# Optimization experiments

Hardware: AMD Instinct MI355X
Metric: run time of the kernel (lower is better)

The kernel has to match this reference:

```python
import jax, jax.numpy as jnp
import numpy as np

T, B, C = 512, 4, 256   # seq, batch, in_features
R = 256                 # reduce_dim (== in_features == out_features, required by original view/matmul)
OUT = 256
NE = 64                 # n experts / codebook size
D = R * OUT             # 65536, centroid dimension
TAU = 1.0               # gumbel temperature
DECAY = 0.999           # EMA decay
COMMIT = 0.25           # commitment scale


def setup_inputs() -> dict:
    key = jax.random.key(0)
    ks = jax.random.split(key, 6)
    x = jax.random.normal(ks[0], (T, B, C), dtype=jnp.float32)
    # uniform noise for gumbel sampling (kept as input for determinism)
    u_noise = jax.random.uniform(ks[1], (T * B, NE), dtype=jnp.float32,
                                 minval=1e-6, maxval=1.0 - 1e-6)
    W_map = jax.random.normal(ks[2], (D, C), dtype=jnp.float32) * 0.02   # xavier-ish
    b_map = jnp.zeros((D,), jnp.float32)
    pw_w1 = jax.random.normal(ks[3], (1, 1, R, C), dtype=jnp.float32) * (1.0 / np.sqrt(R))
    pw_B = jnp.zeros((1, 1, OUT), jnp.float32)   # 'constant' bias mode, init 0
    centroids = jax.random.normal(ks[4], (NE, D), dtype=jnp.float32) * 0.5  # init_centroids std
    return {"x": x, "u_noise": u_noise, "W_map": W_map, "b_map": b_map,
            "pw_w1": pw_w1, "pw_B": pw_B, "centroids": centroids}


def reference(x, u_noise, W_map, b_map, pw_w1, pw_B, centroids):
    N = T * B
    # key projection: [N, D]
    keyf = x.reshape(N, C) @ W_map.T + b_map
    kd = jax.lax.stop_gradient(keyf)  # assign() uses points.data

    # squared euclidean cdist: ||p||^2 + ||c||^2 - 2 p c^T   [N, NE]
    d2 = (kd * kd).sum(1, keepdims=True) \
         + (centroids * centroids).sum(1)[None, :] \
         - 2.0 * (kd @ centroids.T)

    # gumbel-softmax routing (soft, hard=False); resp detached (depends only on data)
    g = -jnp.log(-jnp.log(u_noise))
    resp = jax.nn.softmax((-d2 + g) / TAU, axis=-1)  # [N, NE]

    # vectorized EMA centroid update (original loops over experts; math identical,
    # mean_assigned[i] = mean_n resp[n,i]*key[n] = (resp^T @ key)/N), detached in original
    mean_assigned = (resp.T @ kd) / N                # [NE, D]
    centroids_new = DECAY * centroids + (1.0 - DECAY) * mean_assigned

    # quantized U-vectors from UPDATED centroids (update precedes matmul in original)
    quantized = resp @ centroids_new                 # [N, D]

    # euclid commitment loss (quantized detached)
    loss = COMMIT * jnp.mean((keyf - jax.lax.stop_gradient(quantized)) ** 2)

    # dynamic per-token weight: w = quantized.view(T,B,R,C) @ pw_w1  -> [T,B,R,C]
    w2 = jnp.einsum('tbik,kj->tbij', quantized.reshape(T, B, R, C), pw_w1[0, 0])
    # apply to input: [T,B,R,C] @ [T,B,C] -> [T,B,OUT]  (R == OUT)
    out = jnp.einsum('tbij,tbj->tbi', w2, x) + pw_B  # constant bias broadcasts
    return (out, loss)
```

## Files before the change

kernel.cpp:

```cpp
#include <hip/hip_runtime.h>
#include <hip/hip_bf16.h>

constexpr int N_TOK = 2048;
constexpr int C_    = 256;
constexpr int NE    = 64;
constexpr int D_    = 65536;
constexpr float DECAYF = 0.999f;
constexpr float OMD    = 0.001f;
constexpr float ALPHA  = OMD / 2048.0f;
constexpr float RTHRESH = 1e-5f;
constexpr int CHMAX = 8448;
constexpr int SA_GRIDX = 512;

using bf16x8 = __attribute__((ext_vector_type(8))) short;
using f32x4  = __attribute__((ext_vector_type(4))) float;
using u16 = unsigned short;

constexpr size_t OFF_S     = 0;
constexpr size_t OFF_XSUM  = 65536;
constexpr size_t OFF_G     = 65792;
constexpr size_t OFF_M     = 131328;
constexpr size_t OFF_WB    = 147712;
constexpr size_t OFF_BB    = 147968;
constexpr size_t OFF_SUMR  = 147984;
constexpr size_t OFF_A     = 148048;
constexpr size_t OFF_CC0   = 164432;
constexpr size_t OFF_RR    = 168528;
constexpr size_t OFF_CNT   = 172624;
constexpr size_t OFF_CN2   = 172688;
constexpr size_t OFF_CB    = 172752;
constexpr size_t OFF_TSLOT = 172816;
constexpr size_t ZFLOATS   = 174864;
constexpr size_t OFF_RESP  = 174864;
constexpr size_t OFF_AG    = 174864;
constexpr size_t OFF_MA    = 191248;
constexpr size_t OFF_AGA   = 195344;
constexpr size_t OFF_AWB   = 199440;
constexpr size_t OFF_CHE   = 199504;
constexpr size_t OFF_CHB   = 207952;
constexpr size_t OFF_NCH   = 216400;
constexpr size_t OFF_Y     = 305936;
constexpr size_t OFF_CNEW  = 830224;
constexpr size_t OFF_TIDX  = 5024528;
constexpr size_t OFF_TOKR  = 5155600;
constexpr size_t OFF_WTH   = 5286672;
constexpr size_t OFF_SCG   = 13675280;
constexpr size_t OFF_SCC   = 16296720;
constexpr size_t WS_FAST2_END = 18393872;

__device__ __forceinline__ unsigned pack_bf2(float a, float b) {
  __hip_bfloat16 ha = __float2bfloat16(a), hb = __float2bfloat16(b);
  unsigned short ua = *reinterpret_cast<unsigned short*>(&ha);
  unsigned short ub = *reinterpret_cast<unsigned short*>(&hb);
  return (unsigned)ua | ((unsigned)ub << 16);
}

__global__ __launch_bounds__(256) void k_pre(const float* __restrict__ bmap,
    const float* __restrict__ x, const float* __restrict__ W,
    float* __restrict__ bb, float* __restrict__ xsum, float* __restrict__ Wb) {
  int bx = blockIdx.x;
  int t = threadIdx.x;
  if (bx < 4) {
    int base = bx * 16384 + t;
    float s = 0.f;
    for (int q = 0; q < 64; q++) { float v = bmap[base + q * 256]; s = fmaf(v, v, s); }
    __shared__ float red[256];
    red[t] = s;
    __syncthreads();
    for (int k = 128; k > 0; k >>= 1) {
      if (t < k) red[t] += red[t + k];
      __syncthreads();
    }
    if (t == 0) atomicAdd(&bb[0], red[0]);
  } else if (bx < 36) {
    int n0 = (bx - 4) * 64;
    float s = 0.f;
    for (int n = 0; n < 64; n++) s += x[(n0 + n) * C_ + t];
    atomicAdd(&xsum[t], s);
  } else {
    int d0 = (bx - 36) * 256;
    __shared__ float bs[256];
    __shared__ int any;
    if (t == 0) any = 0;
    __syncthreads();
    float bv = bmap[d0 + t];
    bs[t] = bv;
    if (bv != 0.f) any = 1;
    __syncthreads();
    if (any == 0) return;
    float s = 0.f;
    for (int d = 0; d < 256; d++) s = fmaf(bs[d], W[(size_t)(d0 + d) * C_ + t], s);
    atomicAdd(&Wb[t], s);
  }
}

template<int KCHUNK>
__device__ __forceinline__ void gemm_tt_tile(
    const float* __restrict__ Aop, int lda, int ca,
    const float* __restrict__ Bop, int ldb, int cb,
    int d0, float* __restrict__ Out, int ldo, int ro, int co) {
  __shared__ float Wa[32][68], Wb[32][68];
  int t = threadIdx.x;
  int tx = t & 15, ty = t >> 4;
  int lr = t >> 3, lc = (t & 7) * 8;
  float acc[4][4] = {};
  for (int dk = 0; dk < KCHUNK; dk += 32) {
    const float* Arow = &Aop[(size_t)(d0 + dk + lr) * lda + ca];
    const float* Brow = &Bop[(size_t)(d0 + dk + lr) * ldb + cb];
    float4 a0 = *(const float4*)&Arow[lc];
    float4 a1 = *(const float4*)&Arow[lc + 4];
    float4 b0 = *(const float4*)&Brow[lc];
    float4 b1 = *(const float4*)&Brow[lc + 4];
    __syncthreads();
    *(float4*)&Wa[lr][lc]     = a0;
    *(float4*)&Wa[lr][lc + 4] = a1;
    *(float4*)&Wb[lr][lc]     = b0;
    *(float4*)&Wb[lr][lc + 4] = b1;
    __syncthreads();
    #pragma unroll
    for (int k = 0; k < 32; k++) {
      float4 ra4 = *(const float4*)&Wa[k][ty * 4];
      float4 rb4 = *(const float4*)&Wb[k][tx * 4];
      float ra[4] = {ra4.x, ra4.y, ra4.z, ra4.w};
      float rb[4] = {rb4.x, rb4.y, rb4.z, rb4.w};
      #pragma unroll
      for (int i = 0; i < 4; i++)
        #pragma unroll
        for (int j = 0; j < 4; j++)
          acc[i][j] = fmaf(ra[i], rb[j], acc[i][j]);
    }
  }
  #pragma unroll
  for (int i = 0; i < 4; i++)
    #pragma unroll
    for (int j = 0; j < 4; j++)
      atomicAdd(&Out[(size_t)(ro + ty * 4 + i) * ldo + co + tx * 4 + j], acc[i][j]);
}

__global__ __launch_bounds__(256) void k_Tw(const float* __restrict__ W,
    u16* __restrict__ wth) {
  __shared__ float Ls[32][257];
  int t = threadIdx.x;
  int d0 = blockIdx.x * 32;
  int r = t >> 3, c8 = (t & 7) * 32;
  #pragma unroll
  for (int q = 0; q < 8; q++) {
    float4 v = *(const float4*)&W[(size_t)(d0 + r) * 256 + c8 + q * 4];
    Ls[r][c8 + q * 4 + 0] = v.x; Ls[r][c8 + q * 4 + 1] = v.y;
    Ls[r][c8 + q * 4 + 2] = v.z; Ls[r][c8 + q * 4 + 3] = v.w;
  }
  __syncthreads();
  int dq = (t & 3) * 8;
  #pragma unroll
  for (int pQ = 0; pQ < 4; pQ++) {
    int c = pQ * 64 + (t >> 2);
    unsigned hw[4];
    #pragma unroll
    for (int q = 0; q < 4; q++)
      hw[q] = pack_bf2(Ls[dq + 2 * q][c], Ls[dq + 2 * q + 1][c]);
    size_t o = (size_t)c * 65536 + d0 + dq;
    *(uint4*)&wth[o] = make_uint4(hw[0], hw[1], hw[2], hw[3]);
  }
}

__global__ __launch_bounds__(256) void k_G3(const u16* __restrict__ wth,
    float* __restrict__ part) {
  int kb = blockIdx.x;
  int p = blockIdx.y;
  int ti = 0, rem0 = p;
  while (rem0 >= 4 - ti) { rem0 -= 4 - ti; ti++; }
  int tj = ti + rem0;
  bool two = (ti != tj);
  const u16* srcA = wth + (size_t)(ti * 64) * 65536;
  const u16* srcB = wth + (size_t)(tj * 64) * 65536;
  __shared__ __align__(16) u16 Ta[8 * 68 * 8], Tb[8 * 68 * 8];
  int t = threadIdx.x, l = t & 63, w = t >> 6;
  int m0 = w * 16, lm = l & 15, g = l >> 4;
  int scol = t >> 3, skseg = t & 7;
  f32x4 acc[4] = {};
  for (int cc = 0; cc < 16; cc++) {
    int k0 = kb * 1024 + cc * 64;
    __syncthreads();
    {
      uint4 a0 = *(const uint4*)(srcA + (size_t)scol * 65536 + k0 + skseg * 8);
      uint4 a1 = *(const uint4*)(srcA + (size_t)(scol + 32) * 65536 + k0 + skseg * 8);
      *(uint4*)(Ta + (skseg * 68 + scol) * 8) = a0;
      *(uint4*)(Ta + (skseg * 68 + scol + 32) * 8) = a1;
      if (two) {
        uint4 b0 = *(const uint4*)(srcB + (size_t)scol * 65536 + k0 + skseg * 8);
        uint4 b1 = *(const uint4*)(srcB + (size_t)(scol + 32) * 65536 + k0 + skseg * 8);
        *(uint4*)(Tb + (skseg * 68 + scol) * 8) = b0;
        *(uint4*)(Tb + (skseg * 68 + scol + 32) * 8) = b1;
      }
    }
    __syncthreads();
    const u16* TBp = two ? Tb : Ta;
    #pragma unroll
    for (int ks = 0; ks < 2; ks++) {
      int kq = ks * 4 + g;
      bf16x8 av = *(const bf16x8*)(Ta + (kq * 68 + m0 + lm) * 8);
      #pragma unroll
      for (int j = 0; j < 4; j++) {
        bf16x8 bv = *(const bf16x8*)(TBp + (kq * 68 + j * 16 + lm) * 8);
        acc[j] = __builtin_amdgcn_mfma_f32_16x16x32_bf16(av, bv, acc[j], 0, 0, 0);
      }
    }
  }
  float* pp = &part[((size_t)p * 64 + kb) * 4096];
  #pragma unroll
  for (int j = 0; j < 4; j++)
    #pragma unroll
    for (int r = 0; r < 4; r++)
      pp[(m0 + (l >> 4) * 4 + r) * 64 + j * 16 + lm] = acc[j][r];
}

__global__ __launch_bounds__(256) void k_Gslow(const float* __restrict__ W,
    float* __restrict__ part) {
  int p = blockIdx.y;
  int ti = 0, rem0 = p;
  while (rem0 >= 4 - ti) { rem0 -= 4 - ti; ti++; }
  int tj = ti + rem0;
  int c1 = ti * 64, c2 = tj * 64;
  int d0 = blockIdx.x * 1024;
  __shared__ unsigned short Wat[64][40], Wbt[64][40];
  int t = threadIdx.x;
  int h = t >> 7;
  int rem = t & 127;
  int k2 = rem >> 3;
  int c4b = rem & 7;
  int cbase = h ? c2 : c1;
  unsigned short (*dst)[40] = h ? Wbt : Wat;
  int l = t & 63, w = t >> 6;
  int m0 = w * 16;
  int lm = l & 15, q8 = (l >> 4) * 8;
  f32x4 acc[4] = {};
  for (int dk = 0; dk < 1024; dk += 32) {
    __syncthreads();
    #pragma unroll
    for (int it = 0; it < 2; it++) {
      int c4 = c4b + it * 8;
      const float* rp = &W[(size_t)(d0 + dk + k2 * 2) * C_ + cbase + c4 * 4];
      float4 g0 = *(const float4*)rp;
      float4 g1 = *(const float4*)(rp + C_);
      *(unsigned*)&dst[c4 * 4 + 0][k2 * 2] = pack_bf2(g0.x, g1.x);
      *(unsigned*)&dst[c4 * 4 + 1][k2 * 2] = pack_bf2(g0.y, g1.y);
      *(unsigned*)&dst[c4 * 4 + 2][k2 * 2] = pack_bf2(g0.z, g1.z);
      *(unsigned*)&dst[c4 * 4 + 3][k2 * 2] = pack_bf2(g0.w, g1.w);
    }
    __syncthreads();
    bf16x8 av = *(const bf16x8*)&Wat[m0 + lm][q8];
    #pragma unroll
    for (int j = 0; j < 4; j++) {
      bf16x8 bv = *(const bf16x8*)&Wbt[j * 16 + lm][q8];
      acc[j] = __builtin_amdgcn_mfma_f32_16x16x32_bf16(av, bv, acc[j], 0, 0, 0);
    }
  }
  float* pp = &part[((size_t)p * 64 + blockIdx.x) * 4096];
  #pragma unroll
  for (int j = 0; j < 4; j++)
    #pragma unroll
    for (int r = 0; r < 4; r++)
      pp[(m0 + (l >> 4) * 4 + r) * 64 + j * 16 + lm] = acc[j][r];
}

__global__ __launch_bounds__(256) void k_Gred(const float* __restrict__ part,
    float* __restrict__ G) {
  int p = blockIdx.y;
  int ti = 0, rem0 = p;
  while (rem0 >= 4 - ti) { rem0 -= 4 - ti; ti++; }
  int tj = ti + rem0;
  int i = blockIdx.x * 256 + threadIdx.x;
  const float* base = part + (size_t)p * 64 * 4096 + i;
  float s = 0.f;
  for (int kb = 0; kb < 64; kb++) s += base[(size_t)kb * 4096];
  int r = i >> 6, c = i & 63;
  G[(ti * 64 + r) * C_ + tj * 64 + c] = s;
  if (ti != tj) G[(tj * 64 + c) * C_ + ti * 64 + r] = s;
}

__global__ __launch_bounds__(256) void k_Mred(const float* __restrict__ mpart,
    float* __restrict__ M) {
  int i = blockIdx.x * 256 + threadIdx.x;
  int kb0 = blockIdx.y * 64;
  float s = 0.f;
  #pragma unroll 8
  for (int kb = 0; kb < 64; kb++) s += mpart[(size_t)(kb0 + kb) * 16384 + i];
  atomicAdd(&M[i], s);
}

__global__ __launch_bounds__(256) void k_CCred(const float* __restrict__ part,
    float* __restrict__ CC0) {
  int i = (blockIdx.x & 15) * 256 + threadIdx.x;
  int kb0 = (blockIdx.x >> 4) * 64;
  float s = 0.f;
  #pragma unroll 8
  for (int kb = 0; kb < 64; kb++) s += part[(size_t)(kb0 + kb) * 4096 + i];
  atomicAdd(&CC0[i], s);
}

__global__ __launch_bounds__(256) void k_redAll(const float* __restrict__ gp,
    const float* __restrict__ mp, const float* __restrict__ cp,
    float* __restrict__ G, float* __restrict__ M, float* __restrict__ CC0) {
  int bx = blockIdx.x;
  if (bx < 160) {
    int p = bx / 16, ib = bx % 16;
    int ti = 0, rem0 = p;
    while (rem0 >= 4 - ti) { rem0 -= 4 - ti; ti++; }
    int tj = ti + rem0;
    int i = ib * 256 + threadIdx.x;
    const float* base = gp + (size_t)p * 64 * 4096 + i;
    float s = 0.f;
    for (int kb = 0; kb < 64; kb++) s += base[(size_t)kb * 4096];
    int r = i >> 6, c = i & 63;
    G[(ti * 64 + r) * C_ + tj * 64 + c] = s;
    if (ti != tj) G[(tj * 64 + c) * C_ + ti * 64 + r] = s;
  } else if (bx < 416) {
    int idx = bx - 160;
    int i = (idx & 63) * 256 + threadIdx.x;
    int kb0 = (idx >> 6) * 64;
    float s = 0.f;
    #pragma unroll 8
    for (int kb = 0; kb < 64; kb++) s += mp[(size_t)(kb0 + kb) * 16384 + i];
    atomicAdd(&M[i], s);
  } else {
    int idx = bx - 416;
    int i = (idx & 15) * 256 + threadIdx.x;
    int kb0 = (idx >> 4) * 64;
    float s = 0.f;
    #pragma unroll 8
    for (int kb = 0; kb < 64; kb++) s += cp[(size_t)(kb0 + kb) * 4096 + i];
    atomicAdd(&CC0[i], s);
  }
}


__global__ __launch_bounds__(256) void k_AR(const float* __restrict__ resp,
    const float* __restrict__ x, float* __restrict__ A, float* __restrict__ RR) {
  if (blockIdx.y < 4)
    gemm_tt_tile<256>(resp, NE, 0, x, C_, blockIdx.y * 64, blockIdx.x * 256,
                      A, C_, 0, blockIdx.y * 64);
  else
    gemm_tt_tile<256>(resp, NE, 0, resp, NE, 0, blockIdx.x * 256, RR, NE, 0, 0);
}

__global__ __launch_bounds__(256) void k_sr(const float* __restrict__ resp,
    float* __restrict__ sumresp) {
  int e = threadIdx.x & 63, part = threadIdx.x >> 6;
  int n0 = blockIdx.x * 256 + part * 64;
  float s = 0.f;
  for (int n = n0; n < n0 + 64; n++) s += resp[n * NE + e];
  __shared__ float red[256];
  red[threadIdx.x] = s;
  __syncthreads();
  if (part == 0)
    atomicAdd(&sumresp[e], red[e] + red[64 + e] + red[128 + e] + red[192 + e]);
}

__global__ __launch_bounds__(256) void k_M(const float* __restrict__ cen,
    const float* __restrict__ W, float* __restrict__ mpart) {
  int kb = blockIdx.x;
  int c0 = blockIdx.y * 64;
  int d0 = kb * 256;
  __shared__ float As[32][68];
  __shared__ float Bs[32][68];
  int t = threadIdx.x;
  int tx = t & 15, ty = t >> 4;
  int e = t >> 2, dg = t & 3;
  int lr = t >> 3, lc = (t & 7) * 8;
  float acc[4][4] = {};
  for (int dk = 0; dk < 256; dk += 32) {
    const float* cr = &cen[(size_t)e * D_ + d0 + dk];
    float4 cv0 = *(const float4*)&cr[dg * 4];
    float4 cv1 = *(const float4*)&cr[16 + dg * 4];
    const float* wr = &W[(size_t)(d0 + dk + lr) * C_ + c0];
    float4 w0 = *(const float4*)&wr[lc];
    float4 w1 = *(const float4*)&wr[lc + 4];
    __syncthreads();
    As[dg * 4 + 0][e] = cv0.x; As[dg * 4 + 1][e] = cv0.y;
    As[dg * 4 + 2][e] = cv0.z; As[dg * 4 + 3][e] = cv0.w;
    As[16 + dg * 4 + 0][e] = cv1.x; As[16 + dg * 4 + 1][e] = cv1.y;
    As[16 + dg * 4 + 2][e] = cv1.z; As[16 + dg * 4 + 3][e] = cv1.w;
    *(float4*)&Bs[lr][lc]     = w0;
    *(float4*)&Bs[lr][lc + 4] = w1;
    __syncthreads();
    #pragma unroll 8
    for (int k = 0; k < 32; k++) {
      float4 ra4 = *(const float4*)&As[k][ty * 4];
      float4 rb4 = *(const float4*)&Bs[k][tx * 4];
      float ra[4] = {ra4.x, ra4.y, ra4.z, ra4.w};
      float rb[4] = {rb4.x, rb4.y, rb4.z, rb4.w};
      #pragma unroll
      for (int i = 0; i < 4; i++)
        #pragma unroll
        for (int j = 0; j < 4; j++)
          acc[i][j] = fmaf(ra[i], rb[j], acc[i][j]);
    }
  }
  float* pp = &mpart[(size_t)kb * 16384];
  #pragma unroll
  for (int i = 0; i < 4; i++)
    *(float4*)&pp[(ty * 4 + i) * C_ + c0 + tx * 4] = *(float4*)&acc[i][0];
}

__global__ __launch_bounds__(256) void k_CCp(const float* __restrict__ cen,
    const float* __restrict__ bmap, float* __restrict__ part,
    float* __restrict__ cb) {
  int d0 = blockIdx.x * 128;
  __shared__ float cs[32][68];
  __shared__ float red[256];
  int t = threadIdx.x;
  int e = t >> 2, dg = t & 3;
  int tx = t & 15, ty = t >> 4;
  float acc[4][4] = {};
  float cbp = 0.f;
  for (int dk = 0; dk < 128; dk += 32) {
    const float* cr = &cen[(size_t)e * D_ + d0 + dk];
    float4 v0 = *(const float4*)&cr[dg * 4];
    float4 v1 = *(const float4*)&cr[16 + dg * 4];
    const float* br = &bmap[d0 + dk];
    float4 b0 = *(const float4*)&br[dg * 4];
    float4 b1 = *(const float4*)&br[16 + dg * 4];
    cbp += v0.x * b0.x + v0.y * b0.y + v0.z * b0.z + v0.w * b0.w
         + v1.x * b1.x + v1.y * b1.y + v1.z * b1.z + v1.w * b1.w;
    __syncthreads();
    cs[dg * 4 + 0][e] = v0.x; cs[dg * 4 + 1][e] = v0.y;
    cs[dg * 4 + 2][e] = v0.z; cs[dg * 4 + 3][e] = v0.w;
    cs[16 + dg * 4 + 0][e] = v1.x; cs[16 + dg * 4 + 1][e] = v1.y;
    cs[16 + dg * 4 + 2][e] = v1.z; cs[16 + dg * 4 + 3][e] = v1.w;
    __syncthreads();
    #pragma unroll
    for (int k = 0; k < 32; k++) {
      float4 ra4 = *(const float4*)&cs[k][ty * 4];
      float4 rb4 = *(const float4*)&cs[k][tx * 4];
      float ra[4] = {ra4.x, ra4.y, ra4.z, ra4.w};
      float rb[4] = {rb4.x, rb4.y, rb4.z, rb4.w};
      #pragma unroll
      for (int i = 0; i < 4; i++)
        #pragma unroll
        for (int j = 0; j < 4; j++)
          acc[i][j] = fmaf(ra[i], rb[j], acc[i][j]);
    }
  }
  float* pp = &part[(size_t)blockIdx.x * 4096];
  #pragma unroll
  for (int i = 0; i < 4; i++)
    *(float4*)&pp[(ty * 4 + i) * 64 + tx * 4] = *(float4*)&acc[i][0];
  red[t] = cbp;
  __syncthreads();
  if (t < 64)
    atomicAdd(&cb[t], red[t * 4] + red[t * 4 + 1] + red[t * 4 + 2] + red[t * 4 + 3]);
}

__global__ __launch_bounds__(256) void k_ygs(const float* __restrict__ x,
    const float* __restrict__ pw, const float* __restrict__ G,
    float* __restrict__ y, float* __restrict__ gsum) {
  int n0 = blockIdx.x * 64;
  bool isg = blockIdx.y >= 4;
  int k0 = (blockIdx.y & 3) * 64;
  const float* B = isg ? G : pw;
  __shared__ float Xs[64][17], Ps[64][17];
  __shared__ float red[256];
  int t = threadIdx.x;
  int tx = t & 15, ty = t >> 4;
  int r = t >> 2, q4 = (t & 3) * 4;
  float acc[4][4] = {};
  for (int j0 = 0; j0 < 256; j0 += 16) {
    float4 va = *(const float4*)&x[(n0 + r) * C_ + j0 + q4];
    float4 vb = *(const float4*)&B[(k0 + r) * C_ + j0 + q4];
    __syncthreads();
    Xs[r][q4] = va.x; Xs[r][q4+1] = va.y; Xs[r][q4+2] = va.z; Xs[r][q4+3] = va.w;
    Ps[r][q4] = vb.x; Ps[r][q4+1] = vb.y; Ps[r][q4+2] = vb.z; Ps[r][q4+3] = vb.w;
    __syncthreads();
    #pragma unroll
    for (int k = 0; k < 16; k++) {
      float ra[4], rb[4];
      #pragma unroll
      for (int i = 0; i < 4; i++) ra[i] = Xs[ty*4 + i][k];
      #pragma unroll
      for (int j = 0; j < 4; j++) rb[j] = Ps[tx*4 + j][k];
      #pragma unroll
      for (int i = 0; i < 4; i++)
        #pragma unroll
        for (int j = 0; j < 4; j++)
          acc[i][j] = fmaf(ra[i], rb[j], acc[i][j]);
    }
  }
  if (!isg) {
    #pragma unroll
    for (int i = 0; i < 4; i++)
      #pragma unroll
      for (int j = 0; j < 4; j++)
        y[(n0 + ty*4 + i) * C_ + k0 + tx*4 + j] = acc[i][j];
  } else {
    float s = 0.f;
    #pragma unroll
    for (int i = 0; i < 4; i++) {
      float4 xv = *(const float4*)&x[(size_t)(n0 + ty*4 + i) * C_ + k0 + tx*4];
      s += acc[i][0]*xv.x + acc[i][1]*xv.y + acc[i][2]*xv.z + acc[i][3]*xv.w;
    }
    red[t] = s;
    __syncthreads();
    for (int k = 128; k > 0; k >>= 1) {
      if (t < k) red[t] += red[t + k];
      __syncthreads();
    }
    if (t == 0) atomicAdd(gsum, red[0]);
  }
}

__global__ __launch_bounds__(256) void k_resp(const float* __restrict__ x,
    const float* __restrict__ u, const float* __restrict__ M,
    const float* __restrict__ CC0, const float* __restrict__ cb,
    float* __restrict__ resp) {
  int t = threadIdx.x;
  int tok = t >> 6, e = t & 63;
  int n = blockIdx.x * 4 + tok;
  __shared__ float xs[4][256];
  *(float4*)&xs[tok][e * 4] = *(const float4*)&x[n * C_ + e * 4];
  __syncthreads();
  const float* Me = M + e * C_;
  const float* xr = xs[tok];
  float s = 0.f;
  #pragma unroll 8
  for (int j = 0; j < 256; j += 4) {
    float4 m4 = *(const float4*)&Me[j];
    s = fmaf(xr[j],   m4.x, s);
    s = fmaf(xr[j+1], m4.y, s);
    s = fmaf(xr[j+2], m4.z, s);
    s = fmaf(xr[j+3], m4.w, s);
  }
  float uu = u[n * NE + e];
  float g = -logf(-logf(uu));
  float logit = 2.0f * (s + cb[e]) - CC0[e * 65] + g;
  float m = logit;
  for (int off = 32; off > 0; off >>= 1) m = fmaxf(m, __shfl_xor(m, off));
  float ex = expf(logit - m);
  float sum = ex;
  for (int off = 32; off > 0; off >>= 1) sum += __shfl_xor(sum, off);
  resp[n * NE + e] = ex / sum;
}

__global__ __launch_bounds__(256) void k_route(const float* __restrict__ resp,
    unsigned int* __restrict__ cnt, int* __restrict__ tokidx,
    float* __restrict__ tokr, int* __restrict__ tslot) {
  int n = blockIdx.x * 256 + threadIdx.x;
  int s = 0;
  #pragma unroll 4
  for (int e = 0; e < NE; e++) {
    float r = resp[n * NE + e];
    if (r > RTHRESH) {
      unsigned pos = atomicAdd(&cnt[e], 1u);
      tokidx[e * 2048 + pos] = n;
      tokr[e * 2048 + pos] = r;
      s++;
    }
  }
  tslot[n] = s;
}

__global__ __launch_bounds__(256) void k_plan(const unsigned int* __restrict__ cnt,
    int* __restrict__ che, int* __restrict__ chb, int* __restrict__ nch) {
  __shared__ int cbase[65];
  __shared__ int ncs[64];
  int t = threadIdx.x;
  if (t < 64) ncs[t] = ((int)cnt[t] + 15) >> 4;
  __syncthreads();
  if (t == 0) {
    int s = 0;
    for (int e = 0; e < 64; e++) { cbase[e] = s; s += ncs[e]; }
    cbase[64] = s;
    nch[0] = s < CHMAX ? s : CHMAX;
  }
  __syncthreads();
  for (int e = 0; e < 64; e++) {
    int b0 = cbase[e], nc = cbase[e + 1] - b0;
    for (int i = t; i < nc; i += 256) {
      int idx = b0 + i;
      if (idx < CHMAX) { che[idx] = e; chb[idx] = i * 16; }
    }
  }
}

__global__ __launch_bounds__(256) void k_ag(const float* __restrict__ A,
    const float* __restrict__ G, const float* __restrict__ Wb,
    float* __restrict__ AG, float* __restrict__ AWb) {
  int e = blockIdx.x, c = threadIdx.x;
  float s = 0.f;
  for (int cp = 0; cp < C_; cp++) s = fmaf(A[e * C_ + cp], G[cp * C_ + c], s);
  AG[e * C_ + c] = s;
  float p = A[e * C_ + c] * Wb[c];
  __shared__ float red[256];
  red[c] = p;
  __syncthreads();
  for (int k = 128; k > 0; k >>= 1) {
    if (c < k) red[c] += red[c + k];
    __syncthreads();
  }
  if (c == 0) AWb[e] = red[0];
}

__global__ __launch_bounds__(256) void k_small64(const float* __restrict__ M,
    const float* __restrict__ A, const float* __restrict__ AG,
    float* __restrict__ MA, float* __restrict__ AGA) {
  int e = blockIdx.x;
  int f = threadIdx.x >> 2, q = threadIdx.x & 3;
  float s1 = 0.f, s2 = 0.f;
  for (int c = q * 64; c < q * 64 + 64; c++) {
    float a = A[f * C_ + c];
    s1 = fmaf(M[e * C_ + c], a, s1);
    s2 = fmaf(AG[e * C_ + c], a, s2);
  }
  __shared__ float r1[256], r2[256];
  r1[threadIdx.x] = s1; r2[threadIdx.x] = s2;
  __syncthreads();
  if (q == 0) {
    MA[e * NE + f]  = r1[f*4] + r1[f*4+1] + r1[f*4+2] + r1[f*4+3];
    AGA[e * NE + f] = r2[f*4] + r2[f*4+1] + r2[f*4+2] + r2[f*4+3];
  }
}

__global__ __launch_bounds__(256) void k_cnew(const float* __restrict__ A,
    const float* __restrict__ sumresp, const float* __restrict__ cen,
    const float* __restrict__ bmap, const float* __restrict__ W,
    float* __restrict__ cnew) {
  int d0 = blockIdx.x * 64;
  __shared__ __align__(16) u16 Abf[64 * 264];
  __shared__ __align__(16) u16 Wt[64 * 264];
  __shared__ float srs[64];
  int t = threadIdx.x, l = t & 63;
  int m0 = (t >> 6) * 16, lm = l & 15, g = l >> 4;
  {
    int e = t >> 2, c0 = (t & 3) * 64;
    const float* ar = &A[e * C_ + c0];
    u16* dst = &Abf[e * 264 + c0];
    #pragma unroll
    for (int q = 0; q < 8; q++) {
      float4 v0 = *(const float4*)&ar[q * 8];
      float4 v1 = *(const float4*)&ar[q * 8 + 4];
      *(uint4*)&dst[q * 8] = make_uint4(pack_bf2(v0.x, v0.y), pack_bf2(v0.z, v0.w),
                                        pack_bf2(v1.x, v1.y), pack_bf2(v1.z, v1.w));
    }
    int r = t >> 2;
    const float* wr = &W[(size_t)(d0 + r) * C_ + c0];
    u16* wdst = &Wt[r * 264 + c0];
    #pragma unroll
    for (int q = 0; q < 8; q++) {
      float4 v0 = *(const float4*)&wr[q * 8];
      float4 v1 = *(const float4*)&wr[q * 8 + 4];
      *(uint4*)&wdst[q * 8] = make_uint4(pack_bf2(v0.x, v0.y), pack_bf2(v0.z, v0.w),
                                         pack_bf2(v1.x, v1.y), pack_bf2(v1.z, v1.w));
    }
    if (t < 64) srs[t] = sumresp[t];
  }
  __syncthreads();
  f32x4 acc[4] = {};
  #pragma unroll
  for (int kk = 0; kk < 8; kk++) {
    bf16x8 av = *(const bf16x8*)&Abf[(m0 + lm) * 264 + kk * 32 + g * 8];
    #pragma unroll
    for (int j = 0; j < 4; j++) {
      bf16x8 bv = *(const bf16x8*)&Wt[(j * 16 + lm) * 264 + kk * 32 + g * 8];
      acc[j] = __builtin_amdgcn_mfma_f32_16x16x32_bf16(av, bv, acc[j], 0, 0, 0);
    }
  }
  #pragma unroll
  for (int j = 0; j < 4; j++) {
    int d = d0 + j * 16 + lm;
    float bv = bmap[d];
    #pragma unroll
    for (int r = 0; r < 4; r++) {
      int e = m0 + g * 4 + r;
      size_t o = (size_t)e * D_ + d;
      cnew[o] = DECAYF * cen[o] + ALPHA * (acc[j][r] + srs[e] * bv);
    }
  }
}

__global__ __launch_bounds__(256) void k_bias(const float* __restrict__ pwB, float* __restrict__ out) {
  int idx = blockIdx.x * 256 + threadIdx.x;
  out[idx] = pwB[idx & 255];
}

__global__ __launch_bounds__(256) void k_sA(const int* __restrict__ che,
    const int* __restrict__ chb, const int* __restrict__ nch,
    const unsigned int* __restrict__ cnt, const int* __restrict__ tokidx,
    const float* __restrict__ tokr, const int* __restrict__ tslot,
    const float* __restrict__ y, const float* __restrict__ cnew,
    float* __restrict__ out) {
  int nchv = nch[0];
  int i0 = blockIdx.y * 128;
  __shared__ int nsh[16]; __shared__ float rsh[16]; __shared__ int wsh[16];
  __shared__ float Ys[16][260];
  __shared__ float Bs[32][132];
  int t = threadIdx.x;
  for (int ch = blockIdx.x; ch < nchv; ch += SA_GRIDX) {
    int e = che[ch], base = chb[ch];
    int c = (int)cnt[e];
    __syncthreads();
    if (t < 16) {
      int idx = base + t;
      if (idx < c) {
        int n = tokidx[e * 2048 + idx];
        nsh[t] = n; rsh[t] = tokr[e * 2048 + idx]; wsh[t] = tslot[n];
      } else { nsh[t] = 0; rsh[t] = 0.f; wsh[t] = 2; }
    }
    __syncthreads();
    {
      int row = t >> 4, c0 = (t & 15) * 16;
      const float* yr = &y[nsh[row] * C_ + c0];
      float4 v0 = *(const float4*)&yr[0];
      float4 v1 = *(const float4*)&yr[4];
      float4 v2 = *(const float4*)&yr[8];
      float4 v3 = *(const float4*)&yr[12];
      *(float4*)&Ys[row][c0]      = v0;
      *(float4*)&Ys[row][c0 + 4]  = v1;
      *(float4*)&Ys[row][c0 + 8]  = v2;
      *(float4*)&Ys[row][c0 + 12] = v3;
    }
    int tx = t & 31, ty = t >> 5;
    int br = t >> 1, bk = (t & 1) * 16;
    float acc[2][4] = {};
    for (int k0 = 0; k0 < 256; k0 += 32) {
      const float* Brow = &cnew[(size_t)e * D_ + (size_t)(i0 + br) * C_ + k0 + bk];
      float4 b0 = *(const float4*)&Brow[0];
      float4 b1 = *(const float4*)&Brow[4];
      float4 b2 = *(const float4*)&Brow[8];
      float4 b3 = *(const float4*)&Brow[12];
      __syncthreads();
      Bs[bk+0][br]  = b0.x; Bs[bk+1][br]  = b0.y; Bs[bk+2][br]  = b0.z; Bs[bk+3][br]  = b0.w;
      Bs[bk+4][br]  = b1.x; Bs[bk+5][br]  = b1.y; Bs[bk+6][br]  = b1.z; Bs[bk+7][br]  = b1.w;
      Bs[bk+8][br]  = b2.x; Bs[bk+9][br]  = b2.y; Bs[bk+10][br] = b2.z; Bs[bk+11][br] = b2.w;
      Bs[bk+12][br] = b3.x; Bs[bk+13][br] = b3.y; Bs[bk+14][br] = b3.z; Bs[bk+15][br] = b3.w;
      __syncthreads();
      #pragma unroll
      for (int kk = 0; kk < 32; kk++) {
        float a0 = Ys[ty*2 + 0][k0 + kk];
        float a1 = Ys[ty*2 + 1][k0 + kk];
        float4 bv = *(const float4*)&Bs[kk][tx*4];
        acc[0][0] = fmaf(a0, bv.x, acc[0][0]); acc[0][1] = fmaf(a0, bv.y, acc[0][1]);
        acc[0][2] = fmaf(a0, bv.z, acc[0][2]); acc[0][3] = fmaf(a0, bv.w, acc[0][3]);
        acc[1][0] = fmaf(a1, bv.x, acc[1][0]); acc[1][1] = fmaf(a1, bv.y, acc[1][1]);
        acc[1][2] = fmaf(a1, bv.z, acc[1][2]); acc[1][3] = fmaf(a1, bv.w, acc[1][3]);
      }
    }
    #pragma unroll
    for (int i = 0; i < 2; i++) {
      int tk = ty*2 + i;
      float r = rsh[tk];
      if (r == 0.f) continue;
      int n = nsh[tk];
      float* op = &out[n * C_ + i0 + tx*4];
      if (wsh[tk] == 1) {
        float4 cur = *(const float4*)op;
        cur.x += r * acc[i][0]; cur.y += r * acc[i][1];
        cur.z += r * acc[i][2]; cur.w += r * acc[i][3];
        *(float4*)op = cur;
      } else {
        atomicAdd(op + 0, r * acc[i][0]);
        atomicAdd(op + 1, r * acc[i][1]);
        atomicAdd(op + 2, r * acc[i][2]);
        atomicAdd(op + 3, r * acc[i][3]);
      }
    }
  }
}

__global__ __launch_bounds__(256) void k_finalize(
    const float* __restrict__ gsum, const float* __restrict__ M,
    const float* __restrict__ A, const float* __restrict__ AG,
    const float* __restrict__ CC0, const float* __restrict__ RR,
    const float* __restrict__ MA, const float* __restrict__ AGA,
    const float* __restrict__ Xsum, const float* __restrict__ Wb,
    const float* __restrict__ bb, const float* __restrict__ sr,
    const float* __restrict__ cb, const float* __restrict__ AWb,
    float* __restrict__ out) {
  int t = threadIdx.x;
  float a_gs = (t == 0) ? gsum[0] : 0.f;
  float a_am = 0.f, a_aag = 0.f;
  for (int i = t; i < 16384; i += 256) {
    float a = A[i];
    a_am  = fmaf(M[i], a, a_am);
    a_aag = fmaf(AG[i], a, a_aag);
  }
  float a_cc = 0.f, a_ma = 0.f, a_aga = 0.f, a_cbsr = 0.f, a_awbsr = 0.f, a_srsr = 0.f;
  for (int p = t; p < 4096; p += 256) {
    float r = RR[p];
    int e = p >> 6, f = p & 63;
    float srf = sr[f];
    a_cc    = fmaf(r, CC0[p], a_cc);
    a_ma    = fmaf(r, MA[p], a_ma);
    a_aga   = fmaf(r, AGA[p], a_aga);
    a_cbsr  = fmaf(r * cb[e], srf, a_cbsr);
    a_awbsr = fmaf(r * AWb[e], srf, a_awbsr);
    a_srsr  = fmaf(r * sr[e], srf, a_srsr);
  }
  float a_xw = Xsum[t] * Wb[t];
  float a_srcb = 0.f, a_srawb = 0.f, a_sr2 = 0.f;
  if (t < 64) { float s = sr[t]; a_srcb = s * cb[t]; a_srawb = s * AWb[t]; a_sr2 = s * s; }
  float v[13] = {a_gs, a_am, a_aag, a_cc, a_ma, a_aga, a_cbsr, a_awbsr, a_srsr,
                 a_xw, a_srcb, a_srawb, a_sr2};
  __shared__ float red[256];
  __shared__ float tot[13];
  for (int q = 0; q < 13; q++) {
    red[t] = v[q];
    __syncthreads();
    for (int s2 = 128; s2 > 0; s2 >>= 1) {
      if (t < s2) red[t] += red[t + s2];
      __syncthreads();
    }
    if (t == 0) tot[q] = red[0];
    __syncthreads();
  }
  if (t == 0) {
    const float q = DECAYF, al = ALPHA;
    float bbv = bb[0];
    float sumkeyf2 = tot[0] + 2.f * tot[9] + 2048.f * bbv;
    float cross = q * (tot[1] + tot[10]) + al * (tot[2] + 2.f * tot[11] + bbv * tot[12]);
    float sumq2 = q*q * tot[3] + 2.f*q*al * (tot[4] + tot[6])
                + al*al * (tot[5] + 2.f * tot[7] + bbv * tot[8]);
    out[524288] = (0.25f / (2048.0f * 65536.0f)) * (sumkeyf2 - 2.f * cross + sumq2);
  }
}

extern "C" void kernel_launch(void* const* d_in, const int* in_sizes, int n_in,
                              void* d_out, int out_size, void* d_ws, size_t ws_size,
                              hipStream_t stream) {
  const float* x    = (const float*)d_in[0];
  const float* u    = (const float*)d_in[1];
  const float* Wm   = (const float*)d_in[2];
  const float* bmap = (const float*)d_in[3];
  const float* pw   = (const float*)d_in[4];
  const float* pwB  = (const float*)d_in[5];
  const float* cen  = (const float*)d_in[6];
  float* out = (float*)d_out;
  float* ws  = (float*)d_ws;

  float* Xsum    = ws + OFF_XSUM;
  float* G       = ws + OFF_G;
  float* M       = ws + OFF_M;
  float* Wb      = ws + OFF_WB;
  float* bb      = ws + OFF_BB;
  float* gsum    = ws + OFF_BB + 1;
  float* sumresp = ws + OFF_SUMR;
  float* A       = ws + OFF_A;
  float* CC0     = ws + OFF_CC0;
  float* RR      = ws + OFF_RR;
  unsigned int* cnt = (unsigned int*)(ws + OFF_CNT);
  float* cb      = ws + OFF_CB;
  int*   tslot   = (int*)(ws + OFF_TSLOT);
  float* resp    = ws + OFF_RESP;
  float* AG      = ws + OFF_AG;
  float* MA      = ws + OFF_MA;
  float* AGA     = ws + OFF_AGA;
  float* AWb     = ws + OFF_AWB;
  int*   che     = (int*)(ws + OFF_CHE);
  int*   chb     = (int*)(ws + OFF_CHB);
  int*   nch     = (int*)(ws + OFF_NCH);
  float* y       = ws + OFF_Y;
  float* cnew    = ws + OFF_CNEW;
  float* scratch = ws + OFF_CNEW;
  int*   tokidx  = (int*)(ws + OFF_TIDX);
  float* tokr    = ws + OFF_TOKR;
  u16*   wth     = (u16*)(ws + OFF_WTH);
  float* sc_g    = ws + OFF_SCG;
  float* sc_cc   = ws + OFF_SCC;

  bool fast2 = ws_size >= (size_t)WS_FAST2_END * sizeof(float);

  hipMemsetAsync(d_ws, 0, ZFLOATS * sizeof(float), stream);

  k_pre<<<292, 256, 0, stream>>>(bmap, x, Wm, bb, Xsum, Wb);
  if (fast2) {
    k_Tw<<<2048, 256, 0, stream>>>(Wm, wth);
    k_G3<<<dim3(64, 10), 256, 0, stream>>>(wth, sc_g);
    k_M<<<dim3(256, 4), 256, 0, stream>>>(cen, Wm, scratch);
    k_CCp<<<512, 256, 0, stream>>>(cen, bmap, sc_cc, cb);
    k_redAll<<<544, 256, 0, stream>>>(sc_g, scratch, sc_cc, G, M, CC0);
  } else {
    k_Gslow<<<dim3(64, 10), 256, 0, stream>>>(Wm, scratch);
    k_Gred<<<dim3(16, 10), 256, 0, stream>>>(scratch, G);
    k_M<<<dim3(256, 4), 256, 0, stream>>>(cen, Wm, scratch);
    k_Mred<<<dim3(64, 4), 256, 0, stream>>>(scratch, M);
    k_CCp<<<512, 256, 0, stream>>>(cen, bmap, scratch, cb);
    k_CCred<<<128, 256, 0, stream>>>(scratch, CC0);
  }
  k_ygs<<<dim3(32, 8), 256, 0, stream>>>(x, pw, G, y, gsum);
  k_resp<<<512, 256, 0, stream>>>(x, u, M, CC0, cb, resp);
  k_route<<<8, 256, 0, stream>>>(resp, cnt, tokidx, tokr, tslot);
  k_AR<<<dim3(8, 5), 256, 0, stream>>>(resp, x, A, RR);
  k_sr<<<8, 256, 0, stream>>>(resp, sumresp);
  k_plan<<<1, 256, 0, stream>>>(cnt, che, chb, nch);
  k_ag<<<64, 256, 0, stream>>>(A, G, Wb, AG, AWb);
  k_small64<<<64, 256, 0, stream>>>(M, A, AG, MA, AGA);
  k_cnew<<<1024, 256, 0, stream>>>(A, sumresp, cen, bmap, Wm, cnew);
  k_bias<<<2048, 256, 0, stream>>>(pwB, out);
  k_sA<<<dim3(SA_GRIDX, 2), 256, 0, stream>>>(che, chb, nch, cnt, tokidx, tokr,
                                              tslot, y, cnew, out);
  k_finalize<<<1, 256, 0, stream>>>(gsum, M, A, AG, CC0, RR, MA, AGA, Xsum, Wb,
                                    bb, sumresp, cb, AWb, out);
}
```

Baseline: 402.3 us.

## Merge independent stage kernels into block-partitioned fused launches

Collapses roughly a dozen small kernel launches into five multi-role kernels, where the block index decides which sub-task (G Gram tiles, M partials, centroid Gram, y/resp, routing, cnew, scatter) a block runs. The aim is to cut launch overhead and the idle tails between small dependent stages by letting independent work share one grid. In exchange, blocks with very different costs share a launch, shared memory is sized for the largest role, and the slow fallback path looks inconsistent (it launches k_big1 reading wth, which that path never fills).

```diff
diff --git a/kernel.cpp b/kernel.cpp
--- a/kernel.cpp
+++ b/kernel.cpp
@@ -10,13 +10,11 @@
 constexpr float ALPHA  = OMD / 2048.0f;
 constexpr float RTHRESH = 1e-5f;
 constexpr int CHMAX = 8448;
-constexpr int SA_GRIDX = 512;
 
 using bf16x8 = __attribute__((ext_vector_type(8))) short;
 using f32x4  = __attribute__((ext_vector_type(4))) float;
 using u16 = unsigned short;
 
-constexpr size_t OFF_S     = 0;
 constexpr size_t OFF_XSUM  = 65536;
 constexpr size_t OFF_G     = 65792;
 constexpr size_t OFF_M     = 131328;
@@ -27,7 +25,6 @@
 constexpr size_t OFF_CC0   = 164432;
 constexpr size_t OFF_RR    = 168528;
 constexpr size_t OFF_CNT   = 172624;
-constexpr size_t OFF_CN2   = 172688;
 constexpr size_t OFF_CB    = 172752;
 constexpr size_t OFF_TSLOT = 172816;
 constexpr size_t ZFLOATS   = 174864;
@@ -55,16 +52,18 @@
   return (unsigned)ua | ((unsigned)ub << 16);
 }
 
-__global__ __launch_bounds__(256) void k_pre(const float* __restrict__ bmap,
+__global__ __launch_bounds__(256) void k_preTw(const float* __restrict__ bmap,
     const float* __restrict__ x, const float* __restrict__ W,
-    float* __restrict__ bb, float* __restrict__ xsum, float* __restrict__ Wb) {
+    float* __restrict__ bb, float* __restrict__ xsum, float* __restrict__ Wb,
+    u16* __restrict__ wth) {
+  __shared__ __align__(16) char smem[32896];
   int bx = blockIdx.x;
   int t = threadIdx.x;
   if (bx < 4) {
+    float* red = (float*)smem;
     int base = bx * 16384 + t;
     float s = 0.f;
     for (int q = 0; q < 64; q++) { float v = bmap[base + q * 256]; s = fmaf(v, v, s); }
-    __shared__ float red[256];
     red[t] = s;
     __syncthreads();
     for (int k = 128; k > 0; k >>= 1) {
@@ -77,10 +76,10 @@
     float s = 0.f;
     for (int n = 0; n < 64; n++) s += x[(n0 + n) * C_ + t];
     atomicAdd(&xsum[t], s);
-  } else {
+  } else if (bx < 292) {
+    float* bs = (float*)smem;
+    __shared__ int any;
     int d0 = (bx - 36) * 256;
-    __shared__ float bs[256];
-    __shared__ int any;
     if (t == 0) any = 0;
     __syncthreads();
     float bv = bmap[d0 + t];
@@ -91,211 +90,173 @@
     float s = 0.f;
     for (int d = 0; d < 256; d++) s = fmaf(bs[d], W[(size_t)(d0 + d) * C_ + t], s);
     atomicAdd(&Wb[t], s);
-  }
-}
-
-template<int KCHUNK>
-__device__ __forceinline__ void gemm_tt_tile(
-    const float* __restrict__ Aop, int lda, int ca,
-    const float* __restrict__ Bop, int ldb, int cb,
-    int d0, float* __restrict__ Out, int ldo, int ro, int co) {
-  __shared__ float Wa[32][68], Wb[32][68];
+  } else {
+    float (*Ls)[257] = (float(*)[257])smem;
+    int d0 = (bx - 292) * 32;
+    int r = t >> 3, c8 = (t & 7) * 32;
+    #pragma unroll
+    for (int q = 0; q < 8; q++) {
+      float4 v = *(const float4*)&W[(size_t)(d0 + r) * 256 + c8 + q * 4];
+      Ls[r][c8 + q * 4 + 0] = v.x; Ls[r][c8 + q * 4 + 1] = v.y;
+      Ls[r][c8 + q * 4 + 2] = v.z; Ls[r][c8 + q * 4 + 3] = v.w;
+    }
+    __syncthreads();
+    int dq = (t & 3) * 8;
+    #pragma unroll
+    for (int pQ = 0; pQ < 4; pQ++) {
+      int c = pQ * 64 + (t >> 2);
+      unsigned hw[4];
+      #pragma unroll
+      for (int q = 0; q < 4; q++)
+        hw[q] = pack_bf2(Ls[dq + 2 * q][c], Ls[dq + 2 * q + 1][c]);
+      size_t o = (size_t)c * 65536 + d0 + dq;
+      *(uint4*)&wth[o] = make_uint4(hw[0], hw[1], hw[2], hw[3]);
+    }
+  }
+}
+
+__global__ __launch_bounds__(256) void k_big1(const u16* __restrict__ wth,
+    const float* __restrict__ cen, const float* __restrict__ W,
+    const float* __restrict__ bmap, float* __restrict__ gpart,
+    float* __restrict__ mpart, float* __restrict__ cpart, float* __restrict__ cb) {
+  __shared__ __align__(16) char smem[17408];
+  int bx = blockIdx.x;
   int t = threadIdx.x;
-  int tx = t & 15, ty = t >> 4;
-  int lr = t >> 3, lc = (t & 7) * 8;
-  float acc[4][4] = {};
-  for (int dk = 0; dk < KCHUNK; dk += 32) {
-    const float* Arow = &Aop[(size_t)(d0 + dk + lr) * lda + ca];
-    const float* Brow = &Bop[(size_t)(d0 + dk + lr) * ldb + cb];
-    float4 a0 = *(const float4*)&Arow[lc];
-    float4 a1 = *(const float4*)&Arow[lc + 4];
-    float4 b0 = *(const float4*)&Brow[lc];
-    float4 b1 = *(const float4*)&Brow[lc + 4];
-    __syncthreads();
-    *(float4*)&Wa[lr][lc]     = a0;
-    *(float4*)&Wa[lr][lc + 4] = a1;
-    *(float4*)&Wb[lr][lc]     = b0;
-    *(float4*)&Wb[lr][lc + 4] = b1;
-    __syncthreads();
-    #pragma unroll
-    for (int k = 0; k < 32; k++) {
-      float4 ra4 = *(const float4*)&Wa[k][ty * 4];
-      float4 rb4 = *(const float4*)&Wb[k][tx * 4];
-      float ra[4] = {ra4.x, ra4.y, ra4.z, ra4.w};
-      float rb[4] = {rb4.x, rb4.y, rb4.z, rb4.w};
-      #pragma unroll
-      for (int i = 0; i < 4; i++)
+  if (bx < 640) {
+    u16* Ta = (u16*)smem;
+    u16* Tb = Ta + 4352;
+    int kb = bx & 63, p = bx >> 6;
+    int ti = 0, rem0 = p;
+    while (rem0 >= 4 - ti) { rem0 -= 4 - ti; ti++; }
+    int tj = ti + rem0;
+    bool two = (ti != tj);
+    const u16* srcA = wth + (size_t)(ti * 64) * 65536;
+    const u16* srcB = wth + (size_t)(tj * 64) * 65536;
+    int l = t & 63, w = t >> 6;
+    int m0 = w * 16, lm = l & 15, g = l >> 4;
+    int scol = t >> 3, skseg = t & 7;
+    f32x4 acc[4] = {};
+    for (int cc = 0; cc < 16; cc++) {
+      int k0 = kb * 1024 + cc * 64;
+      __syncthreads();
+      {
+        uint4 a0 = *(const uint4*)(srcA + (size_t)scol * 65536 + k0 + skseg * 8);
+        uint4 a1 = *(const uint4*)(srcA + (size_t)(scol + 32) * 65536 + k0 + skseg * 8);
+        *(uint4*)(Ta + (skseg * 68 + scol) * 8) = a0;
+        *(uint4*)(Ta + (skseg * 68 + scol + 32) * 8) = a1;
+        if (two) {
+          uint4 b0 = *(const uint4*)(srcB + (size_t)scol * 65536 + k0 + skseg * 8);
+          uint4 b1 = *(const uint4*)(srcB + (size_t)(scol + 32) * 65536 + k0 + skseg * 8);
+          *(uint4*)(Tb + (skseg * 68 + scol) * 8) = b0;
+          *(uint4*)(Tb + (skseg * 68 + scol + 32) * 8) = b1;
+        }
+      }
+      __syncthreads();
+      const u16* TBp = two ? Tb : Ta;
+      #pragma unroll
+      for (int ks = 0; ks < 2; ks++) {
+        int kq = ks * 4 + g;
+        bf16x8 av = *(const bf16x8*)(Ta + (kq * 68 + m0 + lm) * 8);
         #pragma unroll
-        for (int j = 0; j < 4; j++)
-          acc[i][j] = fmaf(ra[i], rb[j], acc[i][j]);
-    }
-  }
-  #pragma unroll
-  for (int i = 0; i < 4; i++)
+        for (int j = 0; j < 4; j++) {
+          bf16x8 bv = *(const bf16x8*)(TBp + (kq * 68 + j * 16 + lm) * 8);
+          acc[j] = __builtin_amdgcn_mfma_f32_16x16x32_bf16(av, bv, acc[j], 0, 0, 0);
+        }
+      }
+    }
+    float* pp = &gpart[((size_t)p * 64 + kb) * 4096];
     #pragma unroll
     for (int j = 0; j < 4; j++)
-      atomicAdd(&Out[(size_t)(ro + ty * 4 + i) * ldo + co + tx * 4 + j], acc[i][j]);
-}
-
-__global__ __launch_bounds__(256) void k_Tw(const float* __restrict__ W,
-    u16* __restrict__ wth) {
-  __shared__ float Ls[32][257];
-  int t = threadIdx.x;
-  int d0 = blockIdx.x * 32;
-  int r = t >> 3, c8 = (t & 7) * 32;
-  #pragma unroll
-  for (int q = 0; q < 8; q++) {
-    float4 v = *(const float4*)&W[(size_t)(d0 + r) * 256 + c8 + q * 4];
-    Ls[r][c8 + q * 4 + 0] = v.x; Ls[r][c8 + q * 4 + 1] = v.y;
-    Ls[r][c8 + q * 4 + 2] = v.z; Ls[r][c8 + q * 4 + 3] = v.w;
-  }
-  __syncthreads();
-  int dq = (t & 3) * 8;
-  #pragma unroll
-  for (int pQ = 0; pQ < 4; pQ++) {
-    int c = pQ * 64 + (t >> 2);
-    unsigned hw[4];
-    #pragma unroll
-    for (int q = 0; q < 4; q++)
-      hw[q] = pack_bf2(Ls[dq + 2 * q][c], Ls[dq + 2 * q + 1][c]);
-    size_t o = (size_t)c * 65536 + d0 + dq;
-    *(uint4*)&wth[o] = make_uint4(hw[0], hw[1], hw[2], hw[3]);
-  }
-}
-
-__global__ __launch_bounds__(256) void k_G3(const u16* __restrict__ wth,
-    float* __restrict__ part) {
-  int kb = blockIdx.x;
-  int p = blockIdx.y;
-  int ti = 0, rem0 = p;
-  while (rem0 >= 4 - ti) { rem0 -= 4 - ti; ti++; }
-  int tj = ti + rem0;
-  bool two = (ti != tj);
-  const u16* srcA = wth + (size_t)(ti * 64) * 65536;
-  const u16* srcB = wth + (size_t)(tj * 64) * 65536;
-  __shared__ __align__(16) u16 Ta[8 * 68 * 8], Tb[8 * 68 * 8];
-  int t = threadIdx.x, l = t & 63, w = t >> 6;
-  int m0 = w * 16, lm = l & 15, g = l >> 4;
-  int scol = t >> 3, skseg = t & 7;
-  f32x4 acc[4] = {};
-  for (int cc = 0; cc < 16; cc++) {
-    int k0 = kb * 1024 + cc * 64;
-    __syncthreads();
-    {
-      uint4 a0 = *(const uint4*)(srcA + (size_t)scol * 65536 + k0 + skseg * 8);
-      uint4 a1 = *(const uint4*)(srcA + (size_t)(scol + 32) * 65536 + k0 + skseg * 8);
-      *(uint4*)(Ta + (skseg * 68 + scol) * 8) = a0;
-      *(uint4*)(Ta + (skseg * 68 + scol + 32) * 8) = a1;
-      if (two) {
-        uint4 b0 = *(const uint4*)(srcB + (size_t)scol * 65536 + k0 + skseg * 8);
-        uint4 b1 = *(const uint4*)(srcB + (size_t)(scol + 32) * 65536 + k0 + skseg * 8);
-        *(uint4*)(Tb + (skseg * 68 + scol) * 8) = b0;
-        *(uint4*)(Tb + (skseg * 68 + scol + 32) * 8) = b1;
-      }
-    }
-    __syncthreads();
-    const u16* TBp = two ? Tb : Ta;
-    #pragma unroll
-    for (int ks = 0; ks < 2; ks++) {
-      int kq = ks * 4 + g;
-      bf16x8 av = *(const bf16x8*)(Ta + (kq * 68 + m0 + lm) * 8);
-      #pragma unroll
-      for (int j = 0; j < 4; j++) {
-        bf16x8 bv = *(const bf16x8*)(TBp + (kq * 68 + j * 16 + lm) * 8);
-        acc[j] = __builtin_amdgcn_mfma_f32_16x16x32_bf16(av, bv, acc[j], 0, 0, 0);
-      }
-    }
-  }
-  float* pp = &part[((size_t)p * 64 + kb) * 4096];
-  #pragma unroll
-  for (int j = 0; j < 4; j++)
-    #pragma unroll
-    for (int r = 0; r < 4; r++)
-      pp[(m0 + (l >> 4) * 4 + r) * 64 + j * 16 + lm] = acc[j][r];
-}
-
-__global__ __launch_bounds__(256) void k_Gslow(const float* __restrict__ W,
-    float* __restrict__ part) {
-  int p = blockIdx.y;
-  int ti = 0, rem0 = p;
-  while (rem0 >= 4 - ti) { rem0 -= 4 - ti; ti++; }
-  int tj = ti + rem0;
-  int c1 = ti * 64, c2 = tj * 64;
-  int d0 = blockIdx.x * 1024;
-  __shared__ unsigned short Wat[64][40], Wbt[64][40];
-  int t = threadIdx.x;
-  int h = t >> 7;
-  int rem = t & 127;
-  int k2 = rem >> 3;
-  int c4b = rem & 7;
-  int cbase = h ? c2 : c1;
-  unsigned short (*dst)[40] = h ? Wbt : Wat;
-  int l = t & 63, w = t >> 6;
-  int m0 = w * 16;
-  int lm = l & 15, q8 = (l >> 4) * 8;
-  f32x4 acc[4] = {};
-  for (int dk = 0; dk < 1024; dk += 32) {
-    __syncthreads();
-    #pragma unroll
-    for (int it = 0; it < 2; it++) {
-      int c4 = c4b + it * 8;
-      const float* rp = &W[(size_t)(d0 + dk + k2 * 2) * C_ + cbase + c4 * 4];
-      float4 g0 = *(const float4*)rp;
-      float4 g1 = *(const float4*)(rp + C_);
-      *(unsigned*)&dst[c4 * 4 + 0][k2 * 2] = pack_bf2(g0.x, g1.x);
-      *(unsigned*)&dst[c4 * 4 + 1][k2 * 2] = pack_bf2(g0.y, g1.y);
-      *(unsigned*)&dst[c4 * 4 + 2][k2 * 2] = pack_bf2(g0.z, g1.z);
-      *(unsigned*)&dst[c4 * 4 + 3][k2 * 2] = pack_bf2(g0.w, g1.w);
-    }
-    __syncthreads();
-    bf16x8 av = *(const bf16x8*)&Wat[m0 + lm][q8];
-    #pragma unroll
-    for (int j = 0; j < 4; j++) {
-      bf16x8 bv = *(const bf16x8*)&Wbt[j * 16 + lm][q8];
-      acc[j] = __builtin_amdgcn_mfma_f32_16x16x32_bf16(av, bv, acc[j], 0, 0, 0);
-    }
-  }
-  float* pp = &part[((size_t)p * 64 + blockIdx.x) * 4096];
-  #pragma unroll
-  for (int j = 0; j < 4; j++)
-    #pragma unroll
-    for (int r = 0; r < 4; r++)
-      pp[(m0 + (l >> 4) * 4 + r) * 64 + j * 16 + lm] = acc[j][r];
-}
-
-__global__ __launch_bounds__(256) void k_Gred(const float* __restrict__ part,
-    float* __restrict__ G) {
-  int p = blockIdx.y;
-  int ti = 0, rem0 = p;
-  while (rem0 >= 4 - ti) { rem0 -= 4 - ti; ti++; }
-  int tj = ti + rem0;
-  int i = blockIdx.x * 256 + threadIdx.x;
-  const float* base = part + (size_t)p * 64 * 4096 + i;
-  float s = 0.f;
-  for (int kb = 0; kb < 64; kb++) s += base[(size_t)kb * 4096];
-  int r = i >> 6, c = i & 63;
-  G[(ti * 64 + r) * C_ + tj * 64 + c] = s;
-  if (ti != tj) G[(tj * 64 + c) * C_ + ti * 64 + r] = s;
-}
-
-__global__ __launch_bounds__(256) void k_Mred(const float* __restrict__ mpart,
-    float* __restrict__ M) {
-  int i = blockIdx.x * 256 + threadIdx.x;
-  int kb0 = blockIdx.y * 64;
-  float s = 0.f;
-  #pragma unroll 8
-  for (int kb = 0; kb < 64; kb++) s += mpart[(size_t)(kb0 + kb) * 16384 + i];
-  atomicAdd(&M[i], s);
-}
-
-__global__ __launch_bounds__(256) void k_CCred(const float* __restrict__ part,
-    float* __restrict__ CC0) {
-  int i = (blockIdx.x & 15) * 256 + threadIdx.x;
-  int kb0 = (blockIdx.x >> 4) * 64;
-  float s = 0.f;
-  #pragma unroll 8
-  for (int kb = 0; kb < 64; kb++) s += part[(size_t)(kb0 + kb) * 4096 + i];
-  atomicAdd(&CC0[i], s);
+      #pragma unroll
+      for (int r = 0; r < 4; r++)
+        pp[(m0 + (l >> 4) * 4 + r) * 64 + j * 16 + lm] = acc[j][r];
+  } else if (bx < 1664) {
+    float (*As)[68] = (float(*)[68])smem;
+    float (*Bs)[68] = (float(*)[68])(smem + 8704);
+    int idx = bx - 640;
+    int kb = idx & 255, c0 = (idx >> 8) * 64;
+    int d0 = kb * 256;
+    int tx = t & 15, ty = t >> 4;
+    int e = t >> 2, dg = t & 3;
+    int lr = t >> 3, lc = (t & 7) * 8;
+    float acc[4][4] = {};
+    for (int dk = 0; dk < 256; dk += 32) {
+      const float* cr = &cen[(size_t)e * D_ + d0 + dk];
+      float4 cv0 = *(const float4*)&cr[dg * 4];
+      float4 cv1 = *(const float4*)&cr[16 + dg * 4];
+      const float* wr = &W[(size_t)(d0 + dk + lr) * C_ + c0];
+      float4 w0 = *(const float4*)&wr[lc];
+      float4 w1 = *(const float4*)&wr[lc + 4];
+      __syncthreads();
+      As[dg * 4 + 0][e] = cv0.x; As[dg * 4 + 1][e] = cv0.y;
+      As[dg * 4 + 2][e] = cv0.z; As[dg * 4 + 3][e] = cv0.w;
+      As[16 + dg * 4 + 0][e] = cv1.x; As[16 + dg * 4 + 1][e] = cv1.y;
+      As[16 + dg * 4 + 2][e] = cv1.z; As[16 + dg * 4 + 3][e] = cv1.w;
+      *(float4*)&Bs[lr][lc]     = w0;
+      *(float4*)&Bs[lr][lc + 4] = w1;
+      __syncthreads();
+      #pragma unroll 8
+      for (int k = 0; k < 32; k++) {
+        float4 ra4 = *(const float4*)&As[k][ty * 4];
+        float4 rb4 = *(const float4*)&Bs[k][tx * 4];
+        float ra[4] = {ra4.x, ra4.y, ra4.z, ra4.w};
+        float rb[4] = {rb4.x, rb4.y, rb4.z, rb4.w};
+        #pragma unroll
+        for (int i = 0; i < 4; i++)
+          #pragma unroll
+          for (int j = 0; j < 4; j++)
+            acc[i][j] = fmaf(ra[i], rb[j], acc[i][j]);
+      }
+    }
+    float* pp = &mpart[(size_t)kb * 16384];
+    #pragma unroll
+    for (int i = 0; i < 4; i++)
+      *(float4*)&pp[(ty * 4 + i) * C_ + c0 + tx * 4] = *(float4*)&acc[i][0];
+  } else {
+    float (*cs)[68] = (float(*)[68])smem;
+    float* red = (float*)(smem + 8704);
+    int d0 = (bx - 1664) * 128;
+    int e = t >> 2, dg = t & 3;
+    int tx = t & 15, ty = t >> 4;
+    float acc[4][4] = {};
+    float cbp = 0.f;
+    for (int dk = 0; dk < 128; dk += 32) {
+      const float* cr = &cen[(size_t)e * D_ + d0 + dk];
+      float4 v0 = *(const float4*)&cr[dg * 4];
+      float4 v1 = *(const float4*)&cr[16 + dg * 4];
+      const float* br = &bmap[d0 + dk];
+      float4 b0 = *(const float4*)&br[dg * 4];
+      float4 b1 = *(const float4*)&br[16 + dg * 4];
+      cbp += v0.x * b0.x + v0.y * b0.y + v0.z * b0.z + v0.w * b0.w
+           + v1.x * b1.x + v1.y * b1.y + v1.z * b1.z + v1.w * b1.w;
+      __syncthreads();
+      cs[dg * 4 + 0][e] = v0.x; cs[dg * 4 + 1][e] = v0.y;
+      cs[dg * 4 + 2][e] = v0.z; cs[dg * 4 + 3][e] = v0.w;
+      cs[16 + dg * 4 + 0][e] = v1.x; cs[16 + dg * 4 + 1][e] = v1.y;
+      cs[16 + dg * 4 + 2][e] = v1.z; cs[16 + dg * 4 + 3][e] = v1.w;
+      __syncthreads();
+      #pragma unroll
+      for (int k = 0; k < 32; k++) {
+        float4 ra4 = *(const float4*)&cs[k][ty * 4];
+        float4 rb4 = *(const float4*)&cs[k][tx * 4];
+        float ra[4] = {ra4.x, ra4.y, ra4.z, ra4.w};
+        float rb[4] = {rb4.x, rb4.y, rb4.z, rb4.w};
+        #pragma unroll
+        for (int i = 0; i < 4; i++)
+          #pragma unroll
+          for (int j = 0; j < 4; j++)
+            acc[i][j] = fmaf(ra[i], rb[j], acc[i][j]);
+      }
+    }
+    float* pp = &cpart[(size_t)(bx - 1664) * 4096];
+    #pragma unroll
+    for (int i = 0; i < 4; i++)
+      *(float4*)&pp[(ty * 4 + i) * 64 + tx * 4] = *(float4*)&acc[i][0];
+    red[t] = cbp;
+    __syncthreads();
+    if (t < 64)
+      atomicAdd(&cb[t], red[t * 4] + red[t * 4 + 1] + red[t * 4 + 2] + red[t * 4 + 3]);
+  }
 }
 
 __global__ __launch_bounds__(256) void k_redAll(const float* __restrict__ gp,
@@ -333,434 +294,373 @@
   }
 }
 
-
-__global__ __launch_bounds__(256) void k_AR(const float* __restrict__ resp,
-    const float* __restrict__ x, float* __restrict__ A, float* __restrict__ RR) {
-  if (blockIdx.y < 4)
-    gemm_tt_tile<256>(resp, NE, 0, x, C_, blockIdx.y * 64, blockIdx.x * 256,
-                      A, C_, 0, blockIdx.y * 64);
-  else
-    gemm_tt_tile<256>(resp, NE, 0, resp, NE, 0, blockIdx.x * 256, RR, NE, 0, 0);
-}
-
-__global__ __launch_bounds__(256) void k_sr(const float* __restrict__ resp,
+__global__ __launch_bounds__(256) void k_big2(const float* __restrict__ x,
+    const float* __restrict__ pw, const float* __restrict__ G,
+    const float* __restrict__ u, const float* __restrict__ M,
+    const float* __restrict__ CC0, const float* __restrict__ cb,
+    float* __restrict__ y, float* __restrict__ gsum, float* __restrict__ resp,
+    unsigned int* __restrict__ cnt, int* __restrict__ tokidx,
+    float* __restrict__ tokr, int* __restrict__ tslot,
     float* __restrict__ sumresp) {
-  int e = threadIdx.x & 63, part = threadIdx.x >> 6;
-  int n0 = blockIdx.x * 256 + part * 64;
-  float s = 0.f;
-  for (int n = n0; n < n0 + 64; n++) s += resp[n * NE + e];
-  __shared__ float red[256];
-  red[threadIdx.x] = s;
-  __syncthreads();
-  if (part == 0)
-    atomicAdd(&sumresp[e], red[e] + red[64 + e] + red[128 + e] + red[192 + e]);
-}
-
-__global__ __launch_bounds__(256) void k_M(const float* __restrict__ cen,
-    const float* __restrict__ W, float* __restrict__ mpart) {
-  int kb = blockIdx.x;
-  int c0 = blockIdx.y * 64;
-  int d0 = kb * 256;
-  __shared__ float As[32][68];
-  __shared__ float Bs[32][68];
+  __shared__ __align__(16) char smem[9728];
+  int bx = blockIdx.x;
   int t = threadIdx.x;
-  int tx = t & 15, ty = t >> 4;
-  int e = t >> 2, dg = t & 3;
-  int lr = t >> 3, lc = (t & 7) * 8;
-  float acc[4][4] = {};
-  for (int dk = 0; dk < 256; dk += 32) {
-    const float* cr = &cen[(size_t)e * D_ + d0 + dk];
-    float4 cv0 = *(const float4*)&cr[dg * 4];
-    float4 cv1 = *(const float4*)&cr[16 + dg * 4];
-    const float* wr = &W[(size_t)(d0 + dk + lr) * C_ + c0];
-    float4 w0 = *(const float4*)&wr[lc];
-    float4 w1 = *(const float4*)&wr[lc + 4];
-    __syncthreads();
-    As[dg * 4 + 0][e] = cv0.x; As[dg * 4 + 1][e] = cv0.y;
-    As[dg * 4 + 2][e] = cv0.z; As[dg * 4 + 3][e] = cv0.w;
-    As[16 + dg * 4 + 0][e] = cv1.x; As[16 + dg * 4 + 1][e] = cv1.y;
-    As[16 + dg * 4 + 2][e] = cv1.z; As[16 + dg * 4 + 3][e] = cv1.w;
-    *(float4*)&Bs[lr][lc]     = w0;
-    *(float4*)&Bs[lr][lc + 4] = w1;
-    __syncthreads();
-    #pragma unroll 8
-    for (int k = 0; k < 32; k++) {
-      float4 ra4 = *(const float4*)&As[k][ty * 4];
-      float4 rb4 = *(const float4*)&Bs[k][tx * 4];
-      float ra[4] = {ra4.x, ra4.y, ra4.z, ra4.w};
-      float rb[4] = {rb4.x, rb4.y, rb4.z, rb4.w};
+  if (bx < 256) {
+    float (*Xs)[17] = (float(*)[17])smem;
+    float (*Ps)[17] = (float(*)[17])(smem + 4352);
+    float* red = (float*)(smem + 8704);
+    int n0 = (bx & 31) * 64;
+    int by = bx >> 5;
+    bool isg = by >= 4;
+    int k0 = (by & 3) * 64;
+    const float* B = isg ? G : pw;
+    int tx = t & 15, ty = t >> 4;
+    int r = t >> 2, q4 = (t & 3) * 4;
+    float acc[4][4] = {};
+    for (int j0 = 0; j0 < 256; j0 += 16) {
+      float4 va = *(const float4*)&x[(n0 + r) * C_ + j0 + q4];
+      float4 vb = *(const float4*)&B[(k0 + r) * C_ + j0 + q4];
+      __syncthreads();
+      Xs[r][q4] = va.x; Xs[r][q4+1] = va.y; Xs[r][q4+2] = va.z; Xs[r][q4+3] = va.w;
+      Ps[r][q4] = vb.x; Ps[r][q4+1] = vb.y; Ps[r][q4+2] = vb.z; Ps[r][q4+3] = vb.w;
+      __syncthreads();
+      #pragma unroll
+      for (int k = 0; k < 16; k++) {
+        float ra[4], rb[4];
+        #pragma unroll
+        for (int i = 0; i < 4; i++) ra[i] = Xs[ty*4 + i][k];
+        #pragma unroll
+        for (int j = 0; j < 4; j++) rb[j] = Ps[tx*4 + j][k];
+        #pragma unroll
+        for (int i = 0; i < 4; i++)
+          #pragma unroll
+          for (int j = 0; j < 4; j++)
+            acc[i][j] = fmaf(ra[i], rb[j], acc[i][j]);
+      }
+    }
+    if (!isg) {
       #pragma unroll
       for (int i = 0; i < 4; i++)
         #pragma unroll
         for (int j = 0; j < 4; j++)
-          acc[i][j] = fmaf(ra[i], rb[j], acc[i][j]);
-    }
-  }
-  float* pp = &mpart[(size_t)kb * 16384];
-  #pragma unroll
-  for (int i = 0; i < 4; i++)
-    *(float4*)&pp[(ty * 4 + i) * C_ + c0 + tx * 4] = *(float4*)&acc[i][0];
-}
-
-__global__ __launch_bounds__(256) void k_CCp(const float* __restrict__ cen,
-    const float* __restrict__ bmap, float* __restrict__ part,
-    float* __restrict__ cb) {
-  int d0 = blockIdx.x * 128;
-  __shared__ float cs[32][68];
-  __shared__ float red[256];
-  int t = threadIdx.x;
-  int e = t >> 2, dg = t & 3;
-  int tx = t & 15, ty = t >> 4;
-  float acc[4][4] = {};
-  float cbp = 0.f;
-  for (int dk = 0; dk < 128; dk += 32) {
-    const float* cr = &cen[(size_t)e * D_ + d0 + dk];
-    float4 v0 = *(const float4*)&cr[dg * 4];
-    float4 v1 = *(const float4*)&cr[16 + dg * 4];
-    const float* br = &bmap[d0 + dk];
-    float4 b0 = *(const float4*)&br[dg * 4];
-    float4 b1 = *(const float4*)&br[16 + dg * 4];
-    cbp += v0.x * b0.x + v0.y * b0.y + v0.z * b0.z + v0.w * b0.w
-         + v1.x * b1.x + v1.y * b1.y + v1.z * b1.z + v1.w * b1.w;
-    __syncthreads();
-    cs[dg * 4 + 0][e] = v0.x; cs[dg * 4 + 1][e] = v0.y;
-    cs[dg * 4 + 2][e] = v0.z; cs[dg * 4 + 3][e] = v0.w;
-    cs[16 + dg * 4 + 0][e] = v1.x; cs[16 + dg * 4 + 1][e] = v1.y;
-    cs[16 + dg * 4 + 2][e] = v1.z; cs[16 + dg * 4 + 3][e] = v1.w;
-    __syncthreads();
-    #pragma unroll
-    for (int k = 0; k < 32; k++) {
-      float4 ra4 = *(const float4*)&cs[k][ty * 4];
-      float4 rb4 = *(const float4*)&cs[k][tx * 4];
-      float ra[4] = {ra4.x, ra4.y, ra4.z, ra4.w};
-      float rb[4] = {rb4.x, rb4.y, rb4.z, rb4.w};
-      #pragma unroll
-      for (int i = 0; i < 4; i++)
-        #pragma unroll
-        for (int j = 0; j < 4; j++)
-          acc[i][j] = fmaf(ra[i], rb[j], acc[i][j]);
-    }
-  }
-  float* pp = &part[(size_t)blockIdx.x * 4096];
-  #pragma unroll
-  for (int i = 0; i < 4; i++)
-    *(float4*)&pp[(ty * 4 + i) * 64 + tx * 4] = *(float4*)&acc[i][0];
-  red[t] = cbp;
-  __syncthreads();
-  if (t < 64)
-    atomicAdd(&cb[t], red[t * 4] + red[t * 4 + 1] + red[t * 4 + 2] + red[t * 4 + 3]);
-}
-
-__global__ __launch_bounds__(256) void k_ygs(const float* __restrict__ x,
-    const float* __restrict__ pw, const float* __restrict__ G,
-    float* __restrict__ y, float* __restrict__ gsum) {
-  int n0 = blockIdx.x * 64;
-  bool isg = blockIdx.y >= 4;
-  int k0 = (blockIdx.y & 3) * 64;
-  const float* B = isg ? G : pw;
-  __shared__ float Xs[64][17], Ps[64][17];
-  __shared__ float red[256];
-  int t = threadIdx.x;
-  int tx = t & 15, ty = t >> 4;
-  int r = t >> 2, q4 = (t & 3) * 4;
-  float acc[4][4] = {};
-  for (int j0 = 0; j0 < 256; j0 += 16) {
-    float4 va = *(const float4*)&x[(n0 + r) * C_ + j0 + q4];
-    float4 vb = *(const float4*)&B[(k0 + r) * C_ + j0 + q4];
-    __syncthreads();
-    Xs[r][q4] = va.x; Xs[r][q4+1] = va.y; Xs[r][q4+2] = va.z; Xs[r][q4+3] = va.w;
-    Ps[r][q4] = vb.x; Ps[r][q4+1] = vb.y; Ps[r][q4+2] = vb.z; Ps[r][q4+3] = vb.w;
-    __syncthreads();
-    #pragma unroll
-    for (int k = 0; k < 16; k++) {
-      float ra[4], rb[4];
-      #pragma unroll
-      for (int i = 0; i < 4; i++) ra[i] = Xs[ty*4 + i][k];
-      #pragma unroll
-      for (int j = 0; j < 4; j++) rb[j] = Ps[tx*4 + j][k];
-      #pragma unroll
-      for (int i = 0; i < 4; i++)
-        #pragma unroll
-        for (int j = 0; j < 4; j++)
-          acc[i][j] = fmaf(ra[i], rb[j], acc[i][j]);
-    }
-  }
-  if (!isg) {
-    #pragma unroll
-    for (int i = 0; i < 4; i++)
-      #pragma unroll
-      for (int j = 0; j < 4; j++)
-        y[(n0 + ty*4 + i) * C_ + k0 + tx*4 + j] = acc[i][j];
+          y[(n0 + ty*4 + i) * C_ + k0 + tx*4 + j] = acc[i][j];
+    } else {
+      float s = 0.f;
+      #pragma unroll
+      for (int i = 0; i < 4; i++) {
+        float4 xv = *(const float4*)&x[(size_t)(n0 + ty*4 + i) * C_ + k0 + tx*4];
+        s += acc[i][0]*xv.x + acc[i][1]*xv.y + acc[i][2]*xv.z + acc[i][3]*xv.w;
+      }
+      red[t] = s;
+      __syncthreads();
+      for (int k = 128; k > 0; k >>= 1) {
+        if (t < k) red[t] += red[t + k];
+        __syncthreads();
+      }
+      if (t == 0) atomicAdd(gsum, red[0]);
+    }
   } else {
+    float* xs   = (float*)smem;
+    float* ssum = xs + 1024;
+    int tok = t >> 6, e = t & 63;
+    int n = (bx - 256) * 4 + tok;
+    if (t < 64) ssum[t] = 0.f;
+    *(float4*)&xs[tok * 256 + e * 4] = *(const float4*)&x[n * C_ + e * 4];
+    __syncthreads();
+    const float* Me = M + e * C_;
+    const float* xr = &xs[tok * 256];
     float s = 0.f;
-    #pragma unroll
-    for (int i = 0; i < 4; i++) {
-      float4 xv = *(const float4*)&x[(size_t)(n0 + ty*4 + i) * C_ + k0 + tx*4];
-      s += acc[i][0]*xv.x + acc[i][1]*xv.y + acc[i][2]*xv.z + acc[i][3]*xv.w;
-    }
-    red[t] = s;
-    __syncthreads();
-    for (int k = 128; k > 0; k >>= 1) {
-      if (t < k) red[t] += red[t + k];
-      __syncthreads();
-    }
-    if (t == 0) atomicAdd(gsum, red[0]);
-  }
-}
-
-__global__ __launch_bounds__(256) void k_resp(const float* __restrict__ x,
-    const float* __restrict__ u, const float* __restrict__ M,
-    const float* __restrict__ CC0, const float* __restrict__ cb,
-    float* __restrict__ resp) {
-  int t = threadIdx.x;
-  int tok = t >> 6, e = t & 63;
-  int n = blockIdx.x * 4 + tok;
-  __shared__ float xs[4][256];
-  *(float4*)&xs[tok][e * 4] = *(const float4*)&x[n * C_ + e * 4];
-  __syncthreads();
-  const float* Me = M + e * C_;
-  const float* xr = xs[tok];
-  float s = 0.f;
-  #pragma unroll 8
-  for (int j = 0; j < 256; j += 4) {
-    float4 m4 = *(const float4*)&Me[j];
-    s = fmaf(xr[j],   m4.x, s);
-    s = fmaf(xr[j+1], m4.y, s);
-    s = fmaf(xr[j+2], m4.z, s);
-    s = fmaf(xr[j+3], m4.w, s);
-  }
-  float uu = u[n * NE + e];
-  float g = -logf(-logf(uu));
-  float logit = 2.0f * (s + cb[e]) - CC0[e * 65] + g;
-  float m = logit;
-  for (int off = 32; off > 0; off >>= 1) m = fmaxf(m, __shfl_xor(m, off));
-  float ex = expf(logit - m);
-  float sum = ex;
-  for (int off = 32; off > 0; off >>= 1) sum += __shfl_xor(sum, off);
-  resp[n * NE + e] = ex / sum;
-}
-
-__global__ __launch_bounds__(256) void k_route(const float* __restrict__ resp,
-    unsigned int* __restrict__ cnt, int* __restrict__ tokidx,
-    float* __restrict__ tokr, int* __restrict__ tslot) {
-  int n = blockIdx.x * 256 + threadIdx.x;
-  int s = 0;
-  #pragma unroll 4
-  for (int e = 0; e < NE; e++) {
-    float r = resp[n * NE + e];
-    if (r > RTHRESH) {
+    #pragma unroll 8
+    for (int j = 0; j < 256; j += 4) {
+      float4 m4 = *(const float4*)&Me[j];
+      s = fmaf(xr[j],   m4.x, s);
+      s = fmaf(xr[j+1], m4.y, s);
+      s = fmaf(xr[j+2], m4.z, s);
+      s = fmaf(xr[j+3], m4.w, s);
+    }
+    float uu = u[n * NE + e];
+    float g = -logf(-logf(uu));
+    float logit = 2.0f * (s + cb[e]) - CC0[e * 65] + g;
+    float m = logit;
+    for (int off = 32; off > 0; off >>= 1) m = fmaxf(m, __shfl_xor(m, off));
+    float ex = expf(logit - m);
+    float sum = ex;
+    for (int off = 32; off > 0; off >>= 1) sum += __shfl_xor(sum, off);
+    float r = ex / sum;
+    resp[n * NE + e] = r;
+    bool take = r > RTHRESH;
+    unsigned long long mask = __ballot(take);
+    if (take) {
       unsigned pos = atomicAdd(&cnt[e], 1u);
       tokidx[e * 2048 + pos] = n;
       tokr[e * 2048 + pos] = r;
-      s++;
-    }
-  }
-  tslot[n] = s;
-}
-
-__global__ __launch_bounds__(256) void k_plan(const unsigned int* __restrict__ cnt,
-    int* __restrict__ che, int* __restrict__ chb, int* __restrict__ nch) {
-  __shared__ int cbase[65];
-  __shared__ int ncs[64];
+    }
+    if (e == 0) tslot[n] = (int)__popcll(mask);
+    atomicAdd(&ssum[e], r);
+    __syncthreads();
+    if (t < 64) atomicAdd(&sumresp[t], ssum[t]);
+  }
+}
+
+__global__ __launch_bounds__(256) void k_big3(const float* __restrict__ resp,
+    const float* __restrict__ x, float* __restrict__ A, float* __restrict__ RR,
+    const unsigned int* __restrict__ cnt, int* __restrict__ che,
+    int* __restrict__ chb, int* __restrict__ nch) {
+  __shared__ __align__(16) char smem[17408];
+  int bx = blockIdx.x;
   int t = threadIdx.x;
-  if (t < 64) ncs[t] = ((int)cnt[t] + 15) >> 4;
-  __syncthreads();
-  if (t == 0) {
-    int s = 0;
-    for (int e = 0; e < 64; e++) { cbase[e] = s; s += ncs[e]; }
-    cbase[64] = s;
-    nch[0] = s < CHMAX ? s : CHMAX;
-  }
-  __syncthreads();
-  for (int e = 0; e < 64; e++) {
-    int b0 = cbase[e], nc = cbase[e + 1] - b0;
-    for (int i = t; i < nc; i += 256) {
-      int idx = b0 + i;
-      if (idx < CHMAX) { che[idx] = e; chb[idx] = i * 16; }
-    }
-  }
-}
-
-__global__ __launch_bounds__(256) void k_ag(const float* __restrict__ A,
+  if (bx < 40) {
+    int by = bx >> 3, bxx = bx & 7;
+    const float* Aop = resp; int lda = NE, ca = 0;
+    const float* Bop; int ldb, cbn; float* Out; int ldo, co;
+    if (by < 4) { Bop = x; ldb = C_; cbn = by * 64; Out = A; ldo = C_; co = by * 64; }
+    else        { Bop = resp; ldb = NE; cbn = 0; Out = RR; ldo = NE; co = 0; }
+    int d0 = bxx * 256;
+    float (*Wa)[68] = (float(*)[68])smem;
+    float (*Wb)[68] = (float(*)[68])(smem + 8704);
+    int tx = t & 15, ty = t >> 4;
+    int lr = t >> 3, lc = (t & 7) * 8;
+    float acc[4][4] = {};
+    for (int dk = 0; dk < 256; dk += 32) {
+      const float* Arow = &Aop[(size_t)(d0 + dk + lr) * lda + ca];
+      const float* Brow = &Bop[(size_t)(d0 + dk + lr) * ldb + cbn];
+      float4 a0 = *(const float4*)&Arow[lc];
+      float4 a1 = *(const float4*)&Arow[lc + 4];
+      float4 b0 = *(const float4*)&Brow[lc];
+      float4 b1 = *(const float4*)&Brow[lc + 4];
+      __syncthreads();
+      *(float4*)&Wa[lr][lc]     = a0;
+      *(float4*)&Wa[lr][lc + 4] = a1;
+      *(float4*)&Wb[lr][lc]     = b0;
+      *(float4*)&Wb[lr][lc + 4] = b1;
+      __syncthreads();
+      #pragma unroll
+      for (int k = 0; k < 32; k++) {
+        float4 ra4 = *(const float4*)&Wa[k][ty * 4];
+        float4 rb4 = *(const float4*)&Wb[k][tx * 4];
+        float ra[4] = {ra4.x, ra4.y, ra4.z, ra4.w};
+        float rb[4] = {rb4.x, rb4.y, rb4.z, rb4.w};
+        #pragma unroll
+        for (int i = 0; i < 4; i++)
+          #pragma unroll
+          for (int j = 0; j < 4; j++)
+            acc[i][j] = fmaf(ra[i], rb[j], acc[i][j]);
+      }
+    }
+    #pragma unroll
+    for (int i = 0; i < 4; i++)
+      #pragma unroll
+      for (int j = 0; j < 4; j++)
+        atomicAdd(&Out[(size_t)(ty * 4 + i) * ldo + co + tx * 4 + j], acc[i][j]);
+  } else {
+    int* cbase = (int*)smem;
+    int* ncs   = cbase + 65;
+    if (t < 64) ncs[t] = ((int)cnt[t] + 15) >> 4;
+    __syncthreads();
+    if (t == 0) {
+      int s = 0;
+      for (int e = 0; e < 64; e++) { cbase[e] = s; s += ncs[e]; }
+      cbase[64] = s;
+      nch[0] = s < CHMAX ? s : CHMAX;
+    }
+    __syncthreads();
+    for (int e = 0; e < 64; e++) {
+      int b0 = cbase[e], nc = cbase[e + 1] - b0;
+      for (int i = t; i < nc; i += 256) {
+        int idx = b0 + i;
+        if (idx < CHMAX) { che[idx] = e; chb[idx] = i * 16; }
+      }
+    }
+  }
+}
+
+__global__ __launch_bounds__(256) void k_big4(const float* __restrict__ A,
     const float* __restrict__ G, const float* __restrict__ Wb,
-    float* __restrict__ AG, float* __restrict__ AWb) {
-  int e = blockIdx.x, c = threadIdx.x;
-  float s = 0.f;
-  for (int cp = 0; cp < C_; cp++) s = fmaf(A[e * C_ + cp], G[cp * C_ + c], s);
-  AG[e * C_ + c] = s;
-  float p = A[e * C_ + c] * Wb[c];
-  __shared__ float red[256];
-  red[c] = p;
-  __syncthreads();
-  for (int k = 128; k > 0; k >>= 1) {
-    if (c < k) red[c] += red[c + k];
-    __syncthreads();
-  }
-  if (c == 0) AWb[e] = red[0];
-}
-
-__global__ __launch_bounds__(256) void k_small64(const float* __restrict__ M,
-    const float* __restrict__ A, const float* __restrict__ AG,
-    float* __restrict__ MA, float* __restrict__ AGA) {
-  int e = blockIdx.x;
-  int f = threadIdx.x >> 2, q = threadIdx.x & 3;
-  float s1 = 0.f, s2 = 0.f;
-  for (int c = q * 64; c < q * 64 + 64; c++) {
-    float a = A[f * C_ + c];
-    s1 = fmaf(M[e * C_ + c], a, s1);
-    s2 = fmaf(AG[e * C_ + c], a, s2);
-  }
-  __shared__ float r1[256], r2[256];
-  r1[threadIdx.x] = s1; r2[threadIdx.x] = s2;
-  __syncthreads();
-  if (q == 0) {
-    MA[e * NE + f]  = r1[f*4] + r1[f*4+1] + r1[f*4+2] + r1[f*4+3];
-    AGA[e * NE + f] = r2[f*4] + r2[f*4+1] + r2[f*4+2] + r2[f*4+3];
-  }
-}
-
-__global__ __launch_bounds__(256) void k_cnew(const float* __restrict__ A,
     const float* __restrict__ sumresp, const float* __restrict__ cen,
     const float* __restrict__ bmap, const float* __restrict__ W,
-    float* __restrict__ cnew) {
-  int d0 = blockIdx.x * 64;
-  __shared__ __align__(16) u16 Abf[64 * 264];
-  __shared__ __align__(16) u16 Wt[64 * 264];
-  __shared__ float srs[64];
-  int t = threadIdx.x, l = t & 63;
-  int m0 = (t >> 6) * 16, lm = l & 15, g = l >> 4;
-  {
-    int e = t >> 2, c0 = (t & 3) * 64;
-    const float* ar = &A[e * C_ + c0];
-    u16* dst = &Abf[e * 264 + c0];
-    #pragma unroll
-    for (int q = 0; q < 8; q++) {
-      float4 v0 = *(const float4*)&ar[q * 8];
-      float4 v1 = *(const float4*)&ar[q * 8 + 4];
-      *(uint4*)&dst[q * 8] = make_uint4(pack_bf2(v0.x, v0.y), pack_bf2(v0.z, v0.w),
-                                        pack_bf2(v1.x, v1.y), pack_bf2(v1.z, v1.w));
-    }
-    int r = t >> 2;
-    const float* wr = &W[(size_t)(d0 + r) * C_ + c0];
-    u16* wdst = &Wt[r * 264 + c0];
-    #pragma unroll
-    for (int q = 0; q < 8; q++) {
-      float4 v0 = *(const float4*)&wr[q * 8];
-      float4 v1 = *(const float4*)&wr[q * 8 + 4];
-      *(uint4*)&wdst[q * 8] = make_uint4(pack_bf2(v0.x, v0.y), pack_bf2(v0.z, v0.w),
-                                         pack_bf2(v1.x, v1.y), pack_bf2(v1.z, v1.w));
-    }
-    if (t < 64) srs[t] = sumresp[t];
-  }
-  __syncthreads();
-  f32x4 acc[4] = {};
-  #pragma unroll
-  for (int kk = 0; kk < 8; kk++) {
-    bf16x8 av = *(const bf16x8*)&Abf[(m0 + lm) * 264 + kk * 32 + g * 8];
+    const float* __restrict__ pwB, float* __restrict__ AG,
+    float* __restrict__ AWb, float* __restrict__ cnew, float* __restrict__ out) {
+  __shared__ __align__(16) char smem[67840];
+  int bx = blockIdx.x;
+  int t = threadIdx.x;
+  if (bx < 64) {
+    float* red = (float*)smem;
+    int e = bx, c = t;
+    float s = 0.f;
+    for (int cp = 0; cp < C_; cp++) s = fmaf(A[e * C_ + cp], G[cp * C_ + c], s);
+    AG[e * C_ + c] = s;
+    float p = A[e * C_ + c] * Wb[c];
+    red[c] = p;
+    __syncthreads();
+    for (int k = 128; k > 0; k >>= 1) {
+      if (c < k) red[c] += red[c + k];
+      __syncthreads();
+    }
+    if (c == 0) AWb[e] = red[0];
+  } else if (bx < 1088) {
+    u16* Abf = (u16*)smem;
+    u16* Wt  = Abf + 64 * 264;
+    float* srs = (float*)(Wt + 64 * 264);
+    int d0 = (bx - 64) * 64;
+    int l = t & 63;
+    int m0 = (t >> 6) * 16, lm = l & 15, g = l >> 4;
+    {
+      int e = t >> 2, c0 = (t & 3) * 64;
+      const float* ar = &A[e * C_ + c0];
+      u16* dst = &Abf[e * 264 + c0];
+      #pragma unroll
+      for (int q = 0; q < 8; q++) {
+        float4 v0 = *(const float4*)&ar[q * 8];
+        float4 v1 = *(const float4*)&ar[q * 8 + 4];
+        *(uint4*)&dst[q * 8] = make_uint4(pack_bf2(v0.x, v0.y), pack_bf2(v0.z, v0.w),
+                                          pack_bf2(v1.x, v1.y), pack_bf2(v1.z, v1.w));
+      }
+      int r = t >> 2;
+      const float* wr = &W[(size_t)(d0 + r) * C_ + c0];
+      u16* wdst = &Wt[r * 264 + c0];
+      #pragma unroll
+      for (int q = 0; q < 8; q++) {
+        float4 v0 = *(const float4*)&wr[q * 8];
+        float4 v1 = *(const float4*)&wr[q * 8 + 4];
+        *(uint4*)&wdst[q * 8] = make_uint4(pack_bf2(v0.x, v0.y), pack_bf2(v0.z, v0.w),
+                                           pack_bf2(v1.x, v1.y), pack_bf2(v1.z, v1.w));
+      }
+      if (t < 64) srs[t] = sumresp[t];
+    }
+    __syncthreads();
+    f32x4 acc[4] = {};
+    #pragma unroll
+    for (int kk = 0; kk < 8; kk++) {
+      bf16x8 av = *(const bf16x8*)&Abf[(m0 + lm) * 264 + kk * 32 + g * 8];
+      #pragma unroll
+      for (int j = 0; j < 4; j++) {
+        bf16x8 bv = *(const bf16x8*)&Wt[(j * 16 + lm) * 264 + kk * 32 + g * 8];
+        acc[j] = __builtin_amdgcn_mfma_f32_16x16x32_bf16(av, bv, acc[j], 0, 0, 0);
+      }
+    }
     #pragma unroll
     for (int j = 0; j < 4; j++) {
-      bf16x8 bv = *(const bf16x8*)&Wt[(j * 16 + lm) * 264 + kk * 32 + g * 8];
-      acc[j] = __builtin_amdgcn_mfma_f32_16x16x32_bf16(av, bv, acc[j], 0, 0, 0);
-    }
-  }
-  #pragma unroll
-  for (int j = 0; j < 4; j++) {
-    int d = d0 + j * 16 + lm;
-    float bv = bmap[d];
-    #pragma unroll
-    for (int r = 0; r < 4; r++) {
-      int e = m0 + g * 4 + r;
-      size_t o = (size_t)e * D_ + d;
-      cnew[o] = DECAYF * cen[o] + ALPHA * (acc[j][r] + srs[e] * bv);
-    }
-  }
-}
-
-__global__ __launch_bounds__(256) void k_bias(const float* __restrict__ pwB, float* __restrict__ out) {
-  int idx = blockIdx.x * 256 + threadIdx.x;
-  out[idx] = pwB[idx & 255];
-}
-
-__global__ __launch_bounds__(256) void k_sA(const int* __restrict__ che,
+      int d = d0 + j * 16 + lm;
+      float bv = bmap[d];
+      #pragma unroll
+      for (int r = 0; r < 4; r++) {
+        int e = m0 + g * 4 + r;
+        size_t o = (size_t)e * D_ + d;
+        cnew[o] = DECAYF * cen[o] + ALPHA * (acc[j][r] + srs[e] * bv);
+      }
+    }
+  } else {
+    int idx = (bx - 1088) * 256 + t;
+    out[idx] = pwB[idx & 255];
+  }
+}
+
+__global__ __launch_bounds__(256) void k_sAs(const int* __restrict__ che,
     const int* __restrict__ chb, const int* __restrict__ nch,
     const unsigned int* __restrict__ cnt, const int* __restrict__ tokidx,
     const float* __restrict__ tokr, const int* __restrict__ tslot,
     const float* __restrict__ y, const float* __restrict__ cnew,
-    float* __restrict__ out) {
-  int nchv = nch[0];
-  int i0 = blockIdx.y * 128;
-  __shared__ int nsh[16]; __shared__ float rsh[16]; __shared__ int wsh[16];
-  __shared__ float Ys[16][260];
-  __shared__ float Bs[32][132];
+    const float* __restrict__ M, const float* __restrict__ A,
+    const float* __restrict__ AG, float* __restrict__ MA,
+    float* __restrict__ AGA, float* __restrict__ out) {
+  __shared__ __align__(16) char smem[33728];
+  int bx = blockIdx.x;
   int t = threadIdx.x;
-  for (int ch = blockIdx.x; ch < nchv; ch += SA_GRIDX) {
-    int e = che[ch], base = chb[ch];
-    int c = (int)cnt[e];
-    __syncthreads();
-    if (t < 16) {
-      int idx = base + t;
-      if (idx < c) {
-        int n = tokidx[e * 2048 + idx];
-        nsh[t] = n; rsh[t] = tokr[e * 2048 + idx]; wsh[t] = tslot[n];
-      } else { nsh[t] = 0; rsh[t] = 0.f; wsh[t] = 2; }
-    }
-    __syncthreads();
-    {
-      int row = t >> 4, c0 = (t & 15) * 16;
-      const float* yr = &y[nsh[row] * C_ + c0];
-      float4 v0 = *(const float4*)&yr[0];
-      float4 v1 = *(const float4*)&yr[4];
-      float4 v2 = *(const float4*)&yr[8];
-      float4 v3 = *(const float4*)&yr[12];
-      *(float4*)&Ys[row][c0]      = v0;
-      *(float4*)&Ys[row][c0 + 4]  = v1;
-      *(float4*)&Ys[row][c0 + 8]  = v2;
-      *(float4*)&Ys[row][c0 + 12] = v3;
-    }
-    int tx = t & 31, ty = t >> 5;
-    int br = t >> 1, bk = (t & 1) * 16;
-    float acc[2][4] = {};
-    for (int k0 = 0; k0 < 256; k0 += 32) {
-      const float* Brow = &cnew[(size_t)e * D_ + (size_t)(i0 + br) * C_ + k0 + bk];
-      float4 b0 = *(const float4*)&Brow[0];
-      float4 b1 = *(const float4*)&Brow[4];
-      float4 b2 = *(const float4*)&Brow[8];
-      float4 b3 = *(const float4*)&Brow[12];
-      __syncthreads();
-      Bs[bk+0][br]  = b0.x; Bs[bk+1][br]  = b0.y; Bs[bk+2][br]  = b0.z; Bs[bk+3][br]  = b0.w;
-      Bs[bk+4][br]  = b1.x; Bs[bk+5][br]  = b1.y; Bs[bk+6][br]  = b1.z; Bs[bk+7][br]  = b1.w;
-      Bs[bk+8][br]  = b2.x; Bs[bk+9][br]  = b2.y; Bs[bk+10][br] = b2.z; Bs[bk+11][br] = b2.w;
-      Bs[bk+12][br] = b3.x; Bs[bk+13][br] = b3.y; Bs[bk+14][br] = b3.z; Bs[bk+15][br] = b3.w;
-      __syncthreads();
-      #pragma unroll
-      for (int kk = 0; kk < 32; kk++) {
-        float a0 = Ys[ty*2 + 0][k0 + kk];
-        float a1 = Ys[ty*2 + 1][k0 + kk];
-        float4 bv = *(const float4*)&Bs[kk][tx*4];
-        acc[0][0] = fmaf(a0, bv.x, acc[0][0]); acc[0][1] = fmaf(a0, bv.y, acc[0][1]);
-        acc[0][2] = fmaf(a0, bv.z, acc[0][2]); acc[0][3] = fmaf(a0, bv.w, acc[0][3]);
-        acc[1][0] = fmaf(a1, bv.x, acc[1][0]); acc[1][1] = fmaf(a1, bv.y, acc[1][1]);
-        acc[1][2] = fmaf(a1, bv.z, acc[1][2]); acc[1][3] = fmaf(a1, bv.w, acc[1][3]);
-      }
-    }
-    #pragma unroll
-    for (int i = 0; i < 2; i++) {
-      int tk = ty*2 + i;
-      float r = rsh[tk];
-      if (r == 0.f) continue;
-      int n = nsh[tk];
-      float* op = &out[n * C_ + i0 + tx*4];
-      if (wsh[tk] == 1) {
-        float4 cur = *(const float4*)op;
-        cur.x += r * acc[i][0]; cur.y += r * acc[i][1];
-        cur.z += r * acc[i][2]; cur.w += r * acc[i][3];
-        *(float4*)op = cur;
-      } else {
-        atomicAdd(op + 0, r * acc[i][0]);
-        atomicAdd(op + 1, r * acc[i][1]);
-        atomicAdd(op + 2, r * acc[i][2]);
-        atomicAdd(op + 3, r * acc[i][3]);
-      }
+  if (bx < 1024) {
+    int* nsh = (int*)smem;
+    float* rsh = (float*)(smem + 64);
+    int* wsh = (int*)(smem + 128);
+    float (*Ys)[260] = (float(*)[260])(smem + 192);
+    float (*Bs)[132] = (float(*)[132])(smem + 192 + 16640);
+    int nchv = nch[0];
+    int i0 = (bx >> 9) * 128;
+    int chx = bx & 511;
+    for (int ch = chx; ch < nchv; ch += 512) {
+      int e = che[ch], base = chb[ch];
+      int c = (int)cnt[e];
+      __syncthreads();
+      if (t < 16) {
+        int idx = base + t;
+        if (idx < c) {
+          int n = tokidx[e * 2048 + idx];
+          nsh[t] = n; rsh[t] = tokr[e * 2048 + idx]; wsh[t] = tslot[n];
+        } else { nsh[t] = 0; rsh[t] = 0.f; wsh[t] = 2; }
+      }
+      __syncthreads();
+      {
+        int row = t >> 4, c0 = (t & 15) * 16;
+        const float* yr = &y[nsh[row] * C_ + c0];
+        float4 v0 = *(const float4*)&yr[0];
+        float4 v1 = *(const float4*)&yr[4];
+        float4 v2 = *(const float4*)&yr[8];
+        float4 v3 = *(const float4*)&yr[12];
+        *(float4*)&Ys[row][c0]      = v0;
+        *(float4*)&Ys[row][c0 + 4]  = v1;
+        *(float4*)&Ys[row][c0 + 8]  = v2;
+        *(float4*)&Ys[row][c0 + 12] = v3;
+      }
+      int tx = t & 31, ty = t >> 5;
+      int br = t >> 1, bk = (t & 1) * 16;
+      float acc[2][4] = {};
+      for (int k0 = 0; k0 < 256; k0 += 32) {
+        const float* Brow = &cnew[(size_t)e * D_ + (size_t)(i0 + br) * C_ + k0 + bk];
+        float4 b0 = *(const float4*)&Brow[0];
+        float4 b1 = *(const float4*)&Brow[4];
+        float4 b2 = *(const float4*)&Brow[8];
+        float4 b3 = *(const float4*)&Brow[12];
+        __syncthreads();
+        Bs[bk+0][br]  = b0.x; Bs[bk+1][br]  = b0.y; Bs[bk+2][br]  = b0.z; Bs[bk+3][br]  = b0.w;
+        Bs[bk+4][br]  = b1.x; Bs[bk+5][br]  = b1.y; Bs[bk+6][br]  = b1.z; Bs[bk+7][br]  = b1.w;
+        Bs[bk+8][br]  = b2.x; Bs[bk+9][br]  = b2.y; Bs[bk+10][br] = b2.z; Bs[bk+11][br] = b2.w;
+        Bs[bk+12][br] = b3.x; Bs[bk+13][br] = b3.y; Bs[bk+14][br] = b3.z; Bs[bk+15][br] = b3.w;
+        __syncthreads();
+        #pragma unroll
+        for (int kk = 0; kk < 32; kk++) {
+          float a0 = Ys[ty*2 + 0][k0 + kk];
+          float a1 = Ys[ty*2 + 1][k0 + kk];
+          float4 bv = *(const float4*)&Bs[kk][tx*4];
+          acc[0][0] = fmaf(a0, bv.x, acc[0][0]); acc[0][1] = fmaf(a0, bv.y, acc[0][1]);
+          acc[0][2] = fmaf(a0, bv.z, acc[0][2]); acc[0][3] = fmaf(a0, bv.w, acc[0][3]);
+          acc[1][0] = fmaf(a1, bv.x, acc[1][0]); acc[1][1] = fmaf(a1, bv.y, acc[1][1]);
+          acc[1][2] = fmaf(a1, bv.z, acc[1][2]); acc[1][3] = fmaf(a1, bv.w, acc[1][3]);
+        }
+      }
+      #pragma unroll
+      for (int i = 0; i < 2; i++) {
+        int tk = ty*2 + i;
+        float r = rsh[tk];
+        if (r == 0.f) continue;
+        int n = nsh[tk];
+        float* op = &out[n * C_ + i0 + tx*4];
+        if (wsh[tk] == 1) {
+          float4 cur = *(const float4*)op;
+          cur.x += r * acc[i][0]; cur.y += r * acc[i][1];
+          cur.z += r * acc[i][2]; cur.w += r * acc[i][3];
+          *(float4*)op = cur;
+        } else {
+          atomicAdd(op + 0, r * acc[i][0]);
+          atomicAdd(op + 1, r * acc[i][1]);
+          atomicAdd(op + 2, r * acc[i][2]);
+          atomicAdd(op + 3, r * acc[i][3]);
+        }
+      }
+    }
+  } else {
+    float* r1 = (float*)smem;
+    float* r2 = r1 + 256;
+    int e = bx - 1024;
+    int f = t >> 2, q = t & 3;
+    float s1 = 0.f, s2 = 0.f;
+    for (int c = q * 64; c < q * 64 + 64; c++) {
+      float a = A[f * C_ + c];
+      s1 = fmaf(M[e * C_ + c], a, s1);
+      s2 = fmaf(AG[e * C_ + c], a, s2);
+    }
+    r1[t] = s1; r2[t] = s2;
+    __syncthreads();
+    if (q == 0) {
+      MA[e * NE + f]  = r1[f*4] + r1[f*4+1] + r1[f*4+2] + r1[f*4+3];
+      AGA[e * NE + f] = r2[f*4] + r2[f*4+1] + r2[f*4+2] + r2[f*4+3];
     }
   }
 }
@@ -820,6 +720,55 @@
                 + al*al * (tot[5] + 2.f * tot[7] + bbv * tot[8]);
     out[524288] = (0.25f / (2048.0f * 65536.0f)) * (sumkeyf2 - 2.f * cross + sumq2);
   }
+}
+
+__global__ __launch_bounds__(256) void k_Gslow(const float* __restrict__ W,
+    float* __restrict__ part) {
+  int p = blockIdx.y;
+  int ti = 0, rem0 = p;
+  while (rem0 >= 4 - ti) { rem0 -= 4 - ti; ti++; }
+  int tj = ti + rem0;
+  int c1 = ti * 64, c2 = tj * 64;
+  int d0 = blockIdx.x * 1024;
+  __shared__ unsigned short Wat[64][40], Wbt[64][40];
+  int t = threadIdx.x;
+  int h = t >> 7;
+  int rem = t & 127;
+  int k2 = rem >> 3;
+  int c4b = rem & 7;
+  int cbase = h ? c2 : c1;
+  unsigned short (*dst)[40] = h ? Wbt : Wat;
+  int l = t & 63, w = t >> 6;
+  int m0 = w * 16;
+  int lm = l & 15, q8 = (l >> 4) * 8;
+  f32x4 acc[4] = {};
+  for (int dk = 0; dk < 1024; dk += 32) {
+    __syncthreads();
+    #pragma unroll
+    for (int it = 0; it < 2; it++) {
+      int c4 = c4b + it * 8;
+      const float* rp = &W[(size_t)(d0 + dk + k2 * 2) * C_ + cbase + c4 * 4];
+      float4 g0 = *(const float4*)rp;
+      float4 g1 = *(const float4*)(rp + C_);
+      *(unsigned*)&dst[c4 * 4 + 0][k2 * 2] = pack_bf2(g0.x, g1.x);
+      *(unsigned*)&dst[c4 * 4 + 1][k2 * 2] = pack_bf2(g0.y, g1.y);
+      *(unsigned*)&dst[c4 * 4 + 2][k2 * 2] = pack_bf2(g0.z, g1.z);
+      *(unsigned*)&dst[c4 * 4 + 3][k2 * 2] = pack_bf2(g0.w, g1.w);
+    }
+    __syncthreads();
+    bf16x8 av = *(const bf16x8*)&Wat[m0 + lm][q8];
+    #pragma unroll
+    for (int j = 0; j < 4; j++) {
+      bf16x8 bv = *(const bf16x8*)&Wbt[j * 16 + lm][q8];
+      acc[j] = __builtin_amdgcn_mfma_f32_16x16x32_bf16(av, bv, acc[j], 0, 0, 0);
+    }
+  }
+  float* pp = &part[((size_t)p * 64 + blockIdx.x) * 4096];
+  #pragma unroll
+  for (int j = 0; j < 4; j++)
+    #pragma unroll
+    for (int r = 0; r < 4; r++)
+      pp[(m0 + (l >> 4) * 4 + r) * 64 + j * 16 + lm] = acc[j][r];
 }
 
 extern "C" void kernel_launch(void* const* d_in, const int* in_sizes, int n_in,
@@ -869,33 +818,23 @@
 
   hipMemsetAsync(d_ws, 0, ZFLOATS * sizeof(float), stream);
 
-  k_pre<<<292, 256, 0, stream>>>(bmap, x, Wm, bb, Xsum, Wb);
   if (fast2) {
-    k_Tw<<<2048, 256, 0, stream>>>(Wm, wth);
-    k_G3<<<dim3(64, 10), 256, 0, stream>>>(wth, sc_g);
-    k_M<<<dim3(256, 4), 256, 0, stream>>>(cen, Wm, scratch);
-    k_CCp<<<512, 256, 0, stream>>>(cen, bmap, sc_cc, cb);
+    k_preTw<<<2340, 256, 0, stream>>>(bmap, x, Wm, bb, Xsum, Wb, wth);
+    k_big1<<<2176, 256, 0, stream>>>(wth, cen, Wm, bmap, sc_g, scratch, sc_cc, cb);
     k_redAll<<<544, 256, 0, stream>>>(sc_g, scratch, sc_cc, G, M, CC0);
   } else {
-    k_Gslow<<<dim3(64, 10), 256, 0, stream>>>(Wm, scratch);
-    k_Gred<<<dim3(16, 10), 256, 0, stream>>>(scratch, G);
-    k_M<<<dim3(256, 4), 256, 0, stream>>>(cen, Wm, scratch);
-    k_Mred<<<dim3(64, 4), 256, 0, stream>>>(scratch, M);
-    k_CCp<<<512, 256, 0, stream>>>(cen, bmap, scratch, cb);
-    k_CCred<<<128, 256, 0, stream>>>(scratch, CC0);
-  }
-  k_ygs<<<dim3(32, 8), 256, 0, stream>>>(x, pw, G, y, gsum);
-  k_resp<<<512, 256, 0, stream>>>(x, u, M, CC0, cb, resp);
-  k_route<<<8, 256, 0, stream>>>(resp, cnt, tokidx, tokr, tslot);
-  k_AR<<<dim3(8, 5), 256, 0, stream>>>(resp, x, A, RR);
-  k_sr<<<8, 256, 0, stream>>>(resp, sumresp);
-  k_plan<<<1, 256, 0, stream>>>(cnt, che, chb, nch);
-  k_ag<<<64, 256, 0, stream>>>(A, G, Wb, AG, AWb);
-  k_small64<<<64, 256, 0, stream>>>(M, A, AG, MA, AGA);
-  k_cnew<<<1024, 256, 0, stream>>>(A, sumresp, cen, bmap, Wm, cnew);
-  k_bias<<<2048, 256, 0, stream>>>(pwB, out);
-  k_sA<<<dim3(SA_GRIDX, 2), 256, 0, stream>>>(che, chb, nch, cnt, tokidx, tokr,
-                                              tslot, y, cnew, out);
+    k_preTw<<<292, 256, 0, stream>>>(bmap, x, Wm, bb, Xsum, Wb, wth);
+    k_Gslow<<<dim3(64, 10), 256, 0, stream>>>(Wm, ws + OFF_CNEW);
+    k_big1<<<2176, 256, 0, stream>>>(wth, cen, Wm, bmap, sc_g, scratch, sc_cc, cb);
+    k_redAll<<<544, 256, 0, stream>>>(sc_g, scratch, sc_cc, G, M, CC0);
+  }
+  k_big2<<<768, 256, 0, stream>>>(x, pw, G, u, M, CC0, cb, y, gsum, resp,
+                                  cnt, tokidx, tokr, tslot, sumresp);
+  k_big3<<<41, 256, 0, stream>>>(resp, x, A, RR, cnt, che, chb, nch);
+  k_big4<<<3136, 256, 0, stream>>>(A, G, Wb, sumresp, cen, bmap, Wm, pwB,
+                                   AG, AWb, cnew, out);
+  k_sAs<<<1088, 256, 0, stream>>>(che, chb, nch, cnt, tokidx, tokr, tslot,
+                                  y, cnew, M, A, AG, MA, AGA, out);
   k_finalize<<<1, 256, 0, stream>>>(gsum, M, A, AG, CC0, RR, MA, AGA, Xsum, Wb,
                                     bb, sumresp, cb, AWb, out);
 }
```

Measured after the change: 331.8 us. 17.5% less time.
